# Kernel tuning notes

Hardware: AMD Instinct MI355X
Metric: run time of the kernel (lower is better)

Reference implementation:

```python
import jax, jax.numpy as jnp
import numpy as np
from math import pi, log

B, H, W, C = 8, 128, 128, 3
N_LAT, D_LAT = 256, 512
DEPTH = 4
NUM_BANDS = 6
MAX_FREQ = 10.0
BASE = 2.0
CROSS_HEADS, CROSS_DH = 1, 64
LAT_HEADS, LAT_DH = 8, 64
FF_MULT = 4
INPUT_DIM = 2 * (2 * NUM_BANDS + 1) + C  # 29


def setup_inputs():
    ki = iter(jax.random.split(jax.random.key(0), 40))

    def nrm(shape, s=0.02):
        return jax.random.normal(next(ki), shape, jnp.float32) * s

    ic, il = CROSS_HEADS * CROSS_DH, LAT_HEADS * LAT_DH
    d, q = DEPTH, INPUT_DIM
    return {
        "x": jax.random.normal(next(ki), (B, D_LAT), jnp.float32),
        "latents": jax.random.normal(next(ki), (N_LAT, D_LAT), jnp.float32),
        "W_l2l": nrm((D_LAT, N_LAT * D_LAT)),
        "b_l2l": jnp.zeros((N_LAT * D_LAT,), jnp.float32),
        "ca_ln_q_g": jnp.ones((d, q)), "ca_ln_q_b": jnp.zeros((d, q)),
        "ca_ln_c_g": jnp.ones((d, D_LAT)), "ca_ln_c_b": jnp.zeros((d, D_LAT)),
        "ca_Wq": nrm((d, q, ic)), "ca_Wkv": nrm((d, D_LAT, 2 * ic)),
        "ca_Wo": nrm((d, ic, q)), "ca_bo": jnp.zeros((d, q)),
        "cf_ln_g": jnp.ones((d, q)), "cf_ln_b": jnp.zeros((d, q)),
        "cf_W1": nrm((d, q, q * FF_MULT * 2)), "cf_b1": jnp.zeros((d, q * FF_MULT * 2)),
        "cf_W2": nrm((d, q * FF_MULT, q)), "cf_b2": jnp.zeros((d, q)),
        "la_ln_g": jnp.ones((d, D_LAT)), "la_ln_b": jnp.zeros((d, D_LAT)),
        "la_Wq": nrm((d, D_LAT, il)), "la_Wkv": nrm((d, D_LAT, 2 * il)),
        "la_Wo": nrm((d, il, D_LAT)), "la_bo": jnp.zeros((d, D_LAT)),
        "lf_ln_g": jnp.ones((d, D_LAT)), "lf_ln_b": jnp.zeros((d, D_LAT)),
        "lf_W1": nrm((d, D_LAT, D_LAT * FF_MULT * 2)), "lf_b1": jnp.zeros((d, D_LAT * FF_MULT * 2)),
        "lf_W2": nrm((d, D_LAT * FF_MULT, D_LAT)), "lf_b2": jnp.zeros((d, D_LAT)),
    }


def _ln(t, g, b):
    m = jnp.mean(t, -1, keepdims=True)
    v = jnp.mean(jnp.square(t - m), -1, keepdims=True)
    return (t - m) * jax.lax.rsqrt(v + 1e-5) * g + b


def _attn(xq, ctx, Wq, Wkv, Wo, bo, heads):
    dh = Wq.shape[-1] // heads
    b, n, _ = xq.shape
    m = ctx.shape[1]
    qh = (xq @ Wq).reshape(b, n, heads, dh)
    k, v = jnp.split(ctx @ Wkv, 2, axis=-1)
    kh = k.reshape(b, m, heads, dh)
    vh = v.reshape(b, m, heads, dh)
    sim = jnp.einsum('bihd,bjhd->bhij', qh, kh) * (dh ** -0.5)
    attn = jax.nn.softmax(sim, axis=-1)
    out = jnp.einsum('bhij,bjhd->bihd', attn, vh).reshape(b, n, heads * dh)
    return out @ Wo + bo


def _geglu_ff(t, W1, b1, W2, b2):
    a, g = jnp.split(t @ W1 + b1, 2, axis=-1)
    return (a * jax.nn.gelu(g, approximate=False)) @ W2 + b2


def _forward(x, latents, W_l2l, b_l2l, ca_ln_q_g, ca_ln_q_b, ca_ln_c_g, ca_ln_c_b,
             ca_Wq, ca_Wkv, ca_Wo, ca_bo, cf_ln_g, cf_ln_b, cf_W1, cf_b1, cf_W2, cf_b2,
             la_ln_g, la_ln_b, la_Wq, la_Wkv, la_Wo, la_bo,
             lf_ln_g, lf_ln_b, lf_W1, lf_b1, lf_W2, lf_b2):
    # expand latent code to a set of latents and add learned latent array
    lat = (x @ W_l2l + b_l2l).reshape(B, N_LAT, D_LAT) + latents  # (B, N, D)

    # Fourier positional encoding of the output grid
    pos = jnp.stack(jnp.meshgrid(jnp.linspace(-1.0, 1.0, H), jnp.linspace(-1.0, 1.0, W), indexing='ij'), axis=-1)  # (H, W, 2)
    scales = BASE ** jnp.linspace(1.0, log(MAX_FREQ / 2) / log(BASE), NUM_BANDS)  # torch.logspace
    xp = pos[..., None] * scales * pi  # (H, W, 2, NUM_BANDS)
    enc = jnp.concatenate([jnp.sin(xp), jnp.cos(xp), pos[..., None]], axis=-1)  # (H, W, 2, 2B+1)
    enc = enc.reshape(H, W, 2 * (2 * NUM_BANDS + 1)).astype(jnp.float32)

    data = jnp.concatenate([jnp.zeros((B, H, W, C), jnp.float32),
                            jnp.broadcast_to(enc, (B, H, W, enc.shape[-1]))], axis=-1)
    data = data.reshape(B, H * W, INPUT_DIM)

    for i in range(DEPTH):
        ln_lat = _ln(lat, la_ln_g[i], la_ln_b[i])
        lat = lat + _attn(ln_lat, ln_lat, la_Wq[i], la_Wkv[i], la_Wo[i], la_bo[i], LAT_HEADS)
        lat = lat + _geglu_ff(_ln(lat, lf_ln_g[i], lf_ln_b[i]), lf_W1[i], lf_b1[i], lf_W2[i], lf_b2[i])
        qn = _ln(data, ca_ln_q_g[i], ca_ln_q_b[i])
        cn = _ln(lat, ca_ln_c_g[i], ca_ln_c_b[i])
        data = data + _attn(qn, cn, ca_Wq[i], ca_Wkv[i], ca_Wo[i], ca_bo[i], CROSS_HEADS)
        data = data + _geglu_ff(_ln(data, cf_ln_g[i], cf_ln_b[i]), cf_W1[i], cf_b1[i], cf_W2[i], cf_b2[i])

    return data[..., :C].reshape(B, H, W, C)


def reference(x, latents, W_l2l, b_l2l, ca_ln_q_g, ca_ln_q_b, ca_ln_c_g, ca_ln_c_b,
              ca_Wq, ca_Wkv, ca_Wo, ca_bo, cf_ln_g, cf_ln_b, cf_W1, cf_b1, cf_W2, cf_b2,
              la_ln_g, la_ln_b, la_Wq, la_Wkv, la_Wo, la_bo,
              lf_ln_g, lf_ln_b, lf_W1, lf_b1, lf_W2, lf_b2):
    return _forward(x, latents, W_l2l, b_l2l, ca_ln_q_g, ca_ln_q_b, ca_ln_c_g, ca_ln_c_b,
                    ca_Wq, ca_Wkv, ca_Wo, ca_bo, cf_ln_g, cf_ln_b, cf_W1, cf_b1, cf_W2, cf_b2,
                    la_ln_g, la_ln_b, la_Wq, la_Wkv, la_Wo, la_bo,
                    lf_ln_g, lf_ln_b, lf_W1, lf_b1, lf_W2, lf_b2)
```

## Files before the change

kernel.cpp:

```cpp
#include <hip/hip_runtime.h>
#include <math.h>

#define DEV __device__ __forceinline__
#define LSTRIDE 8537088

DEV float gelu_exact(float x){ return 0.5f*x*(1.0f+erff(x*0.70710678118654752440f)); }

DEV unsigned short f2bf(float x){
  union { float f; unsigned int u; } v; v.f = x;
  unsigned int r = v.u + 0x7FFFu + ((v.u >> 16) & 1u);
  return (unsigned short)(r >> 16);
}
DEV float bf2f(unsigned short b){ union { unsigned int u; float f; } v; v.u = ((unsigned int)b)<<16; return v.f; }
DEV void split2(float x, unsigned short& h, unsigned short& l){
  h = f2bf(x); l = f2bf(x - bf2f(h));
}

typedef __bf16 bf16x8 __attribute__((ext_vector_type(8)));
typedef float  f32x4  __attribute__((ext_vector_type(4)));

DEV void gload16(const void* g, void* lds){
  __builtin_amdgcn_global_load_lds((const __attribute__((address_space(1))) unsigned int*)g,
                                   (__attribute__((address_space(3))) unsigned int*)lds, 16, 0, 0);
}

__global__ __launch_bounds__(256) void k_encode(float* __restrict__ data)
{
  int p = blockIdx.x*256 + threadIdx.x;
  int hh = p >> 7, ww = p & 127;
  float y = -1.0f + hh*(2.0f/127.0f);
  float x = -1.0f + ww*(2.0f/127.0f);
  float e[26];
  #pragma unroll
  for (int i=0;i<6;i++){
    float sc = exp2f(1.0f + i*0.26438561897747245f) * 3.14159265358979323846f;
    e[i]     = sinf(y*sc);
    e[6+i]   = cosf(y*sc);
    e[13+i]  = sinf(x*sc);
    e[19+i]  = cosf(x*sc);
  }
  e[12]=y; e[25]=x;
  #pragma unroll
  for (int b=0;b<8;b++){
    float* dr = data + ((size_t)(b*16384 + p))*29;
    dr[0]=0.f; dr[1]=0.f; dr[2]=0.f;
    #pragma unroll
    for (int c=0;c<26;c++) dr[3+c]=e[c];
  }
}

__global__ __launch_bounds__(256) void k_l2l(const float* __restrict__ x,
    const float* __restrict__ Wl, const float* __restrict__ bl,
    const float* __restrict__ latents, float* __restrict__ lat)
{
  __shared__ float xs[8*512];
  int tid = threadIdx.x;
  for (int idx=tid; idx<4096; idx+=256) xs[idx]=x[idx];
  __syncthreads();
  int nIdx = blockIdx.x*256 + tid;
  float acc[8] = {0,0,0,0,0,0,0,0};
  for (int k=0;k<512;k++){
    float w = Wl[(size_t)k*131072 + nIdx];
    #pragma unroll
    for (int m=0;m<8;m++) acc[m] += xs[m*512+k]*w;
  }
  float add = bl[nIdx] + latents[nIdx];
  #pragma unroll
  for (int m=0;m<8;m++) lat[(size_t)m*131072 + nIdx] = acc[m] + add;
}

__global__ __launch_bounds__(256) void k_ln512s(const float* __restrict__ X,
    const float* __restrict__ g, const float* __restrict__ bv,
    unsigned short* __restrict__ hi, unsigned short* __restrict__ lo)
{
  __shared__ float red[8];
  int row = blockIdx.x, tid = threadIdx.x;
  const float* x = X + (size_t)row*512;
  float v0 = x[tid], v1 = x[tid+256];
  float s = v0+v1;
  #pragma unroll
  for (int off=32; off; off>>=1) s += __shfl_xor(s, off);
  if ((tid&63)==0) red[tid>>6] = s;
  __syncthreads();
  float mean = (red[0]+red[1]+red[2]+red[3]) * (1.0f/512.0f);
  float d0 = v0-mean, d1 = v1-mean;
  float q = d0*d0 + d1*d1;
  #pragma unroll
  for (int off=32; off; off>>=1) q += __shfl_xor(q, off);
  if ((tid&63)==0) red[4+(tid>>6)] = q;
  __syncthreads();
  float var = (red[4]+red[5]+red[6]+red[7]) * (1.0f/512.0f);
  float rstd = rsqrtf(var + 1e-5f);
  float y0 = d0*rstd*g[tid]     + bv[tid];
  float y1 = d1*rstd*g[tid+256] + bv[tid+256];
  unsigned short h,l;
  split2(y0,h,l); hi[(size_t)row*512+tid]=h;     lo[(size_t)row*512+tid]=l;
  split2(y1,h,l); hi[(size_t)row*512+tid+256]=h; lo[(size_t)row*512+tid+256]=l;
}

__global__ __launch_bounds__(256) void k_split_w(const float* __restrict__ W,
    unsigned short* __restrict__ hi, int K, int N, int Ntot, int n0off)
{
  __shared__ float t[64][65];
  int z = blockIdx.z;
  W  += (size_t)z*K*N;
  hi += (size_t)z*LSTRIDE;
  unsigned short* lo = hi + (size_t)Ntot*K;
  int k0 = blockIdx.x*64, n0 = blockIdx.y*64;
  int tid = threadIdx.x;
  #pragma unroll
  for (int i=0;i<4;i++){
    int s = tid + 256*i;
    int r = s >> 4, c4 = (s & 15)*4;
    float4 v = *(const float4*)&W[(size_t)(k0+r)*N + n0 + c4];
    t[r][c4+0]=v.x; t[r][c4+1]=v.y; t[r][c4+2]=v.z; t[r][c4+3]=v.w;
  }
  __syncthreads();
  #pragma unroll
  for (int i=0;i<4;i++){
    int s = tid + 256*i;
    int n = s >> 4, kc = (s & 15)*4;
    size_t o = (size_t)(n0off + n0 + n)*K + k0 + kc;
    #pragma unroll
    for (int j=0;j<4;j++){
      unsigned short h,l; split2(t[kc+j][n], h, l);
      hi[o+j]=h; lo[o+j]=l;
    }
  }
}

__global__ __launch_bounds__(256) void k_prep_t(const float* __restrict__ src,
    unsigned short* __restrict__ dst, int K, int N, int Kd, int Nd)
{
  int z = blockIdx.z;
  src += (size_t)z*K*N;
  dst += (size_t)z*LSTRIDE;
  for (int idx = blockIdx.x*256 + threadIdx.x; idx < Nd*Kd; idx += gridDim.x*256){
    int n = idx / Kd, k = idx - n*Kd;
    float v = (k<K && n<N) ? src[(size_t)k*N + n] : 0.f;
    dst[idx] = f2bf(v);
  }
}

__global__ __launch_bounds__(256) void k_prep_w1(const float* __restrict__ W1,
    const float* __restrict__ b1, unsigned short* __restrict__ dst)
{
  int z = blockIdx.z;
  W1  += (size_t)z*6728;
  b1  += (size_t)z*232;
  dst += (size_t)z*LSTRIDE;
  float* b1r = (float*)(dst + 8192);
  for (int idx = blockIdx.x*256 + threadIdx.x; idx < 256*32; idx += gridDim.x*256){
    int n = idx >> 5, k = idx & 31;
    int f = n & 127, isg = n >> 7;
    float v = 0.f;
    if (f < 116 && k < 29) v = W1[(size_t)k*232 + isg*116 + f];
    dst[idx] = f2bf(v);
  }
  int n = blockIdx.x*256 + threadIdx.x;
  if (n < 256){
    int f = n & 127, isg = n >> 7;
    b1r[n] = (f < 116) ? b1[isg*116 + f] : 0.f;
  }
}

__global__ __launch_bounds__(256) void k_mfma(
    const unsigned short* __restrict__ Ahi, const unsigned short* __restrict__ Bhi,
    const float* __restrict__ bias, float* __restrict__ C,
    int M, int N, int K, int Ksplit, int accum)
{
  __shared__ unsigned short sm[4*128*32];
  int tid = threadIdx.x, lane = tid & 63, w = tid >> 6;
  int bm = blockIdx.x*128, bn = blockIdx.y*128;
  int Ks = K / Ksplit;
  int kbeg = blockIdx.z * Ks;
  const unsigned short* tsrc;
  if      (w==0) tsrc = Ahi + (size_t)bm*K;
  else if (w==1) tsrc = Ahi + (size_t)M*K + (size_t)bm*K;
  else if (w==2) tsrc = Bhi + (size_t)bn*K;
  else           tsrc = Bhi + (size_t)N*K + (size_t)bn*K;
  unsigned short* mylds = sm + w*4096;
  f32x4 acc[4][4];
  #pragma unroll
  for(int i=0;i<4;i++)
    #pragma unroll
    for(int j=0;j<4;j++) acc[i][j] = (f32x4){0.f,0.f,0.f,0.f};
  int wm = (w>>1)*64, wn = (w&1)*64;
  int frow = lane & 15, fq = lane >> 4;
  for (int k0 = kbeg; k0 < kbeg + Ks; k0 += 32){
    #pragma unroll
    for (int j=0;j<8;j++){
      int idx = j*64 + lane;
      int row = idx >> 2, qp = idx & 3;
      int q = (qp - row) & 3;
      gload16(tsrc + (size_t)row*K + k0 + q*8, mylds + j*512);
    }
    __syncthreads();
    bf16x8 ah[4], al[4];
    #pragma unroll
    for (int mt=0;mt<4;mt++){
      int row = wm + mt*16 + frow;
      int off = row*32 + ((fq + row)&3)*8;
      ah[mt] = *(const bf16x8*)(sm + off);
      al[mt] = *(const bf16x8*)(sm + 4096 + off);
    }
    #pragma unroll
    for (int nt=0;nt<4;nt++){
      int rowb = wn + nt*16 + frow;
      int offb = rowb*32 + ((fq + rowb)&3)*8;
      bf16x8 bh = *(const bf16x8*)(sm + 2*4096 + offb);
      bf16x8 bl = *(const bf16x8*)(sm + 3*4096 + offb);
      #pragma unroll
      for (int mt=0;mt<4;mt++){
        acc[mt][nt] = __builtin_amdgcn_mfma_f32_16x16x32_bf16(ah[mt], bh, acc[mt][nt], 0,0,0);
        acc[mt][nt] = __builtin_amdgcn_mfma_f32_16x16x32_bf16(ah[mt], bl, acc[mt][nt], 0,0,0);
        acc[mt][nt] = __builtin_amdgcn_mfma_f32_16x16x32_bf16(al[mt], bh, acc[mt][nt], 0,0,0);
      }
    }
    __syncthreads();
  }
  size_t zoff = (size_t)blockIdx.z * ((size_t)M*N);
  #pragma unroll
  for (int mt=0;mt<4;mt++){
    #pragma unroll
    for (int nt=0;nt<4;nt++){
      int col = bn + wn + nt*16 + frow;
      float bv = (bias && blockIdx.z==0) ? bias[col] : 0.f;
      #pragma unroll
      for (int r=0;r<4;r++){
        int row = bm + wm + mt*16 + fq*4 + r;
        float v = acc[mt][nt][r] + bv;
        if (accum) atomicAdd(&C[(size_t)row*N + col], v);
        else       C[zoff + (size_t)row*N + col] = v;
      }
    }
  }
}

__global__ __launch_bounds__(256) void k_mfma_qkv(
    const unsigned short* __restrict__ Ahi, const unsigned short* __restrict__ Bhi,
    float* __restrict__ qout, unsigned short* __restrict__ Kb,
    unsigned short* __restrict__ Vthi, unsigned short* __restrict__ Vtlo,
    int M, int N, int K)
{
  __shared__ unsigned short sm[4*128*32];
  int tid = threadIdx.x, lane = tid & 63, w = tid >> 6;
  int bm = blockIdx.x*128, bn = blockIdx.y*128;
  const unsigned short* tsrc;
  if      (w==0) tsrc = Ahi + (size_t)bm*K;
  else if (w==1) tsrc = Ahi + (size_t)M*K + (size_t)bm*K;
  else if (w==2) tsrc = Bhi + (size_t)bn*K;
  else           tsrc = Bhi + (size_t)N*K + (size_t)bn*K;
  unsigned short* mylds = sm + w*4096;
  f32x4 acc[4][4];
  #pragma unroll
  for(int i=0;i<4;i++)
    #pragma unroll
    for(int j=0;j<4;j++) acc[i][j] = (f32x4){0.f,0.f,0.f,0.f};
  int wm = (w>>1)*64, wn = (w&1)*64;
  int frow = lane & 15, fq = lane >> 4;
  for (int k0 = 0; k0 < K; k0 += 32){
    #pragma unroll
    for (int j=0;j<8;j++){
      int idx = j*64 + lane;
      int row = idx >> 2, qp = idx & 3;
      int q = (qp - row) & 3;
      gload16(tsrc + (size_t)row*K + k0 + q*8, mylds + j*512);
    }
    __syncthreads();
    bf16x8 ah[4], al[4];
    #pragma unroll
    for (int mt=0;mt<4;mt++){
      int row = wm + mt*16 + frow;
      int off = row*32 + ((fq + row)&3)*8;
      ah[mt] = *(const bf16x8*)(sm + off);
      al[mt] = *(const bf16x8*)(sm + 4096 + off);
    }
    #pragma unroll
    for (int nt=0;nt<4;nt++){
      int rowb = wn + nt*16 + frow;
      int offb = rowb*32 + ((fq + rowb)&3)*8;
      bf16x8 bh = *(const bf16x8*)(sm + 2*4096 + offb);
      bf16x8 bl = *(const bf16x8*)(sm + 3*4096 + offb);
      #pragma unroll
      for (int mt=0;mt<4;mt++){
        acc[mt][nt] = __builtin_amdgcn_mfma_f32_16x16x32_bf16(ah[mt], bh, acc[mt][nt], 0,0,0);
        acc[mt][nt] = __builtin_amdgcn_mfma_f32_16x16x32_bf16(ah[mt], bl, acc[mt][nt], 0,0,0);
        acc[mt][nt] = __builtin_amdgcn_mfma_f32_16x16x32_bf16(al[mt], bh, acc[mt][nt], 0,0,0);
      }
    }
    __syncthreads();
  }
  #pragma unroll
  for (int mt=0;mt<4;mt++){
    #pragma unroll
    for (int nt=0;nt<4;nt++){
      int col = bn + wn + nt*16 + frow;
      #pragma unroll
      for (int r=0;r<4;r++){
        int row = bm + wm + mt*16 + fq*4 + r;
        float v = acc[mt][nt][r];
        int b = row >> 8, j = row & 255;
        if (col < 512){
          qout[(size_t)row*512 + col] = v;
        } else if (col < 1024){
          int kc = col - 512, h = kc >> 6, d = kc & 63;
          Kb[((size_t)((b*8+h)*256 + j))*64 + d] = f2bf(v);
        } else {
          int vc = col - 1024, h = vc >> 6, d = vc & 63;
          size_t idx = ((size_t)((b*8+h)*64 + d))*256 + j;
          unsigned short hh,ll; split2(v,hh,ll);
          Vthi[idx]=hh; Vtlo[idx]=ll;
        }
      }
    }
  }
}

__global__ __launch_bounds__(256) void k_mfma_glu(
    const unsigned short* __restrict__ Ahi, const unsigned short* __restrict__ Whi,
    const float* __restrict__ b1, unsigned short* __restrict__ Ghi,
    unsigned short* __restrict__ Glo)
{
  __shared__ unsigned short sm[16384];
  int tid = threadIdx.x, lane = tid & 63, w = tid >> 6;
  int bm = blockIdx.x*128, bnp = blockIdx.y*64;
  const unsigned short* Alo = Ahi + (size_t)2048*512;
  const unsigned short* Wlo = Whi + (size_t)4096*512;
  f32x4 aa[4][2], ag[4][2];
  #pragma unroll
  for (int i=0;i<4;i++)
    #pragma unroll
    for (int j=0;j<2;j++){ aa[i][j]=(f32x4){0.f,0.f,0.f,0.f}; ag[i][j]=(f32x4){0.f,0.f,0.f,0.f}; }
  int wm = (w>>1)*64, wnp = (w&1)*32;
  int frow = lane & 15, fq = lane >> 4;
  for (int k0=0;k0<512;k0+=32){
    #pragma unroll
    for (int j=0;j<8;j++){
      int c0 = w*512 + j*64;
      int c  = c0 + lane;
      int sel = c0 >> 8;
      const unsigned short* src; int wi;
      if (sel < 4){
        src = (sel < 2 ? Ahi : Alo) + (size_t)bm*512;
        wi = c & 511;
      } else {
        const unsigned short* wb = (sel < 6) ? Whi : Wlo;
        int cb = bnp + ((sel & 1) ? 2048 : 0);
        src = wb + (size_t)cb*512;
        wi = c & 255;
      }
      int row = wi >> 2, qp = wi & 3;
      int q = (qp - row) & 3;
      gload16(src + (size_t)row*512 + k0 + q*8, sm + c0*8);
    }
    __syncthreads();
    bf16x8 ah[4], al[4];
    #pragma unroll
    for (int mt=0;mt<4;mt++){
      int r = wm + mt*16 + frow;
      int off = r*32 + ((fq + r)&3)*8;
      ah[mt] = *(const bf16x8*)(sm + off);
      al[mt] = *(const bf16x8*)(sm + 4096 + off);
    }
    #pragma unroll
    for (int nt=0;nt<2;nt++){
      int rb = wnp + nt*16 + frow;
      int offb = rb*32 + ((fq + rb)&3)*8;
      bf16x8 bah = *(const bf16x8*)(sm +  8192 + offb);
      bf16x8 bgh = *(const bf16x8*)(sm + 10240 + offb);
      bf16x8 bal = *(const bf16x8*)(sm + 12288 + offb);
      bf16x8 bgl = *(const bf16x8*)(sm + 14336 + offb);
      #pragma unroll
      for (int mt=0;mt<4;mt++){
        aa[mt][nt] = __builtin_amdgcn_mfma_f32_16x16x32_bf16(ah[mt], bah, aa[mt][nt], 0,0,0);
        aa[mt][nt] = __builtin_amdgcn_mfma_f32_16x16x32_bf16(ah[mt], bal, aa[mt][nt], 0,0,0);
        aa[mt][nt] = __builtin_amdgcn_mfma_f32_16x16x32_bf16(al[mt], bah, aa[mt][nt], 0,0,0);
        ag[mt][nt] = __builtin_amdgcn_mfma_f32_16x16x32_bf16(ah[mt], bgh, ag[mt][nt], 0,0,0);
        ag[mt][nt] = __builtin_amdgcn_mfma_f32_16x16x32_bf16(ah[mt], bgl, ag[mt][nt], 0,0,0);
        ag[mt][nt] = __builtin_amdgcn_mfma_f32_16x16x32_bf16(al[mt], bgh, ag[mt][nt], 0,0,0);
      }
    }
    __syncthreads();
  }
  #pragma unroll
  for (int mt=0;mt<4;mt++){
    #pragma unroll
    for (int nt=0;nt<2;nt++){
      int col = bnp + wnp + nt*16 + frow;
      float ba = b1[col], bg = b1[2048+col];
      #pragma unroll
      for (int r=0;r<4;r++){
        int row = bm + wm + mt*16 + fq*4 + r;
        float av = aa[mt][nt][r] + ba;
        float gv = ag[mt][nt][r] + bg;
        unsigned short h,l; split2(av*gelu_exact(gv), h, l);
        Ghi[(size_t)row*2048 + col] = h;
        Glo[(size_t)row*2048 + col] = l;
      }
    }
  }
}

__global__ __launch_bounds__(256) void k_kvprep(const float* __restrict__ kv, int ld,
    int koff, int voff, int heads, int BH,
    unsigned short* __restrict__ Kb, unsigned short* __restrict__ Vthi,
    unsigned short* __restrict__ Vtlo, int zparts, int zstride)
{
  int total = BH << 14;
  for (int idx = blockIdx.x*256 + threadIdx.x; idx < total; idx += gridDim.x*256){
    int d = idx & 63, j = (idx>>6) & 255, bh = idx >> 14;
    int b = bh / heads, h = bh - b*heads;
    size_t base = ((size_t)(b*256 + j))*ld + koff + h*64 + d;
    float v = 0.f;
    for (int z=0; z<zparts; z++) v += kv[(size_t)z*zstride + base];
    Kb[idx] = f2bf(v);
  }
  for (int idx = blockIdx.x*256 + threadIdx.x; idx < total; idx += gridDim.x*256){
    int j = idx & 255, d = (idx>>8) & 63, bh = idx >> 14;
    int b = bh / heads, h = bh - b*heads;
    size_t base = ((size_t)(b*256 + j))*ld + voff + h*64 + d;
    float v = 0.f;
    for (int z=0; z<zparts; z++) v += kv[(size_t)z*zstride + base];
    if (Vtlo){ unsigned short hh,ll; split2(v,hh,ll); Vthi[idx]=hh; Vtlo[idx]=ll; }
    else Vthi[idx] = f2bf(v);
  }
}

template<int QF32, int SPLITV, int OSPLIT>
__global__ __launch_bounds__(256) void k_attn_mf(
    const void* __restrict__ Qv, const unsigned short* __restrict__ Kb,
    const unsigned short* __restrict__ Vthi, const unsigned short* __restrict__ Vtlo,
    unsigned short* __restrict__ O0, unsigned short* __restrict__ O1,
    int q_rs, int o_rs, int heads, int nper, float scale)
{
  __shared__ unsigned short Pw[4*640];
  int tid = threadIdx.x, lane = tid & 63, w = tid >> 6;
  int l15 = lane & 15, g = lane >> 4;
  int bpb = nper >> 6;
  int bh = blockIdx.x / bpb;
  int q0 = (blockIdx.x - bh*bpb)*64 + w*16;
  int b = bh / heads, h = bh - b*heads;
  bf16x8 aq[2];
  int qrow = b*nper + q0 + l15;
  if (QF32){
    const float* qp = (const float*)Qv + (size_t)qrow*q_rs + h*64 + g*8;
    #pragma unroll
    for (int kt=0;kt<2;kt++){
      bf16x8 v;
      #pragma unroll
      for (int j=0;j<8;j++) v[j] = (__bf16)qp[kt*32 + j];
      aq[kt]=v;
    }
  } else {
    const unsigned short* qp = (const unsigned short*)Qv + (size_t)qrow*q_rs + h*64 + g*8;
    aq[0] = *(const bf16x8*)(qp);
    aq[1] = *(const bf16x8*)(qp + 32);
  }
  const unsigned short* kbb = Kb + ((size_t)bh*256 + l15)*64 + g*8;
  f32x4 sc[16];
  #pragma unroll
  for (int nt=0;nt<16;nt++) sc[nt] = (f32x4){0.f,0.f,0.f,0.f};
  #pragma unroll
  for (int nt=0;nt<16;nt++){
    bf16x8 b0 = *(const bf16x8*)(kbb + (size_t)nt*1024);
    bf16x8 b1 = *(const bf16x8*)(kbb + (size_t)nt*1024 + 32);
    sc[nt] = __builtin_amdgcn_mfma_f32_16x16x32_bf16(aq[0], b0, sc[nt], 0,0,0);
    sc[nt] = __builtin_amdgcn_mfma_f32_16x16x32_bf16(aq[1], b1, sc[nt], 0,0,0);
  }
  float mx[4] = {-1e30f,-1e30f,-1e30f,-1e30f};
  #pragma unroll
  for (int nt=0;nt<16;nt++)
    #pragma unroll
    for (int r=0;r<4;r++){ float v = sc[nt][r]*scale; sc[nt][r]=v; mx[r]=fmaxf(mx[r],v); }
  #pragma unroll
  for (int r=0;r<4;r++){
    #pragma unroll
    for (int m=1;m<16;m<<=1) mx[r] = fmaxf(mx[r], __shfl_xor(mx[r], m));
  }
  float sum[4] = {0.f,0.f,0.f,0.f};
  #pragma unroll
  for (int nt=0;nt<16;nt++)
    #pragma unroll
    for (int r=0;r<4;r++){ float e = __expf(sc[nt][r]-mx[r]); sc[nt][r]=e; sum[r]+=e; }
  #pragma unroll
  for (int r=0;r<4;r++){
    #pragma unroll
    for (int m=1;m<16;m<<=1) sum[r] += __shfl_xor(sum[r], m);
  }
  f32x4 o[4];
  #pragma unroll
  for (int nd=0;nd<4;nd++) o[nd] = (f32x4){0.f,0.f,0.f,0.f};
  unsigned short* pw = Pw + w*640;
  const unsigned short* vb  = Vthi + ((size_t)bh*64 + l15)*256 + g*8;
  const unsigned short* vbl = SPLITV ? (Vtlo + ((size_t)bh*64 + l15)*256 + g*8) : (const unsigned short*)0;
  #pragma unroll
  for (int kt=0;kt<8;kt++){
    __builtin_amdgcn_wave_barrier();
    #pragma unroll
    for (int t2=0;t2<2;t2++){
      int nt = kt*2 + t2;
      #pragma unroll
      for (int r=0;r<4;r++)
        pw[(g*4+r)*40 + t2*16 + l15] = f2bf(sc[nt][r]);
    }
    __builtin_amdgcn_wave_barrier();
    bf16x8 ap = *(const bf16x8*)(pw + l15*40 + g*8);
    #pragma unroll
    for (int nd=0;nd<4;nd++){
      bf16x8 bv = *(const bf16x8*)(vb + (size_t)nd*4096 + kt*32);
      o[nd] = __builtin_amdgcn_mfma_f32_16x16x32_bf16(ap, bv, o[nd], 0,0,0);
      if (SPLITV){
        bf16x8 bl = *(const bf16x8*)(vbl + (size_t)nd*4096 + kt*32);
        o[nd] = __builtin_amdgcn_mfma_f32_16x16x32_bf16(ap, bl, o[nd], 0,0,0);
      }
    }
  }
  float inv[4];
  #pragma unroll
  for (int r=0;r<4;r++) inv[r] = 1.0f/sum[r];
  int orow0 = b*nper + q0;
  #pragma unroll
  for (int nd=0;nd<4;nd++){
    #pragma unroll
    for (int r=0;r<4;r++){
      float v = o[nd][r]*inv[r];
      size_t off = (size_t)(orow0 + g*4 + r)*o_rs + h*64 + nd*16 + l15;
      if (OSPLIT){ unsigned short hh,ll; split2(v,hh,ll); O0[off]=hh; O1[off]=ll; }
      else O0[off] = f2bf(v);
    }
  }
}

__global__ __launch_bounds__(256) void k_cattn(
    const float* __restrict__ X, const float* __restrict__ lng, const float* __restrict__ lnb,
    const unsigned short* __restrict__ WqT, const unsigned short* __restrict__ Kb,
    const unsigned short* __restrict__ Vt, const unsigned short* __restrict__ WoT,
    const float* __restrict__ bo, float* __restrict__ C, float scale)
{
  __shared__ __align__(16) unsigned short qn[64*40];
  __shared__ __align__(16) unsigned short qa[4][16*72];
  int tid = threadIdx.x, lane = tid & 63, w = tid >> 6;
  int l15 = lane & 15, g = lane >> 4;
  int r0 = blockIdx.x*64;
  int bh = r0 >> 14;
  if (tid < 64){
    const float* x = X + (size_t)(r0 + tid)*29;
    float a[29]; float s = 0.f;
    #pragma unroll
    for (int k=0;k<29;k++){ a[k]=x[k]; s+=a[k]; }
    float mean = s*(1.0f/29.0f);
    float qv = 0.f;
    #pragma unroll
    for (int k=0;k<29;k++){ float d=a[k]-mean; qv+=d*d; }
    float rstd = rsqrtf(qv*(1.0f/29.0f) + 1e-5f);
    unsigned short yb[32] __attribute__((aligned(16)));
    #pragma unroll
    for (int k=0;k<29;k++) yb[k] = f2bf((a[k]-mean)*rstd*lng[k] + lnb[k]);
    yb[29]=0; yb[30]=0; yb[31]=0;
    uint4* d4 = (uint4*)(qn + tid*40);
    const uint4* s4 = (const uint4*)yb;
    d4[0]=s4[0]; d4[1]=s4[1]; d4[2]=s4[2]; d4[3]=s4[3];
  }
  __syncthreads();
  int rw = w*16;
  bf16x8 a0 = *(const bf16x8*)(qn + (rw + l15)*40 + g*8);
  f32x4 qv4[4];
  #pragma unroll
  for (int nt=0;nt<4;nt++) qv4[nt] = (f32x4){0.f,0.f,0.f,0.f};
  #pragma unroll
  for (int nt=0;nt<4;nt++){
    bf16x8 bw = *(const bf16x8*)(WqT + (size_t)(nt*16 + l15)*32 + g*8);
    qv4[nt] = __builtin_amdgcn_mfma_f32_16x16x32_bf16(a0, bw, qv4[nt], 0,0,0);
  }
  unsigned short* pa = qa[w];
  #pragma unroll
  for (int nt=0;nt<4;nt++)
    #pragma unroll
    for (int r=0;r<4;r++)
      pa[(g*4+r)*72 + nt*16 + l15] = f2bf(qv4[nt][r]);
  __builtin_amdgcn_wave_barrier();
  bf16x8 aq[2];
  aq[0] = *(const bf16x8*)(pa + l15*72 + g*8);
  aq[1] = *(const bf16x8*)(pa + l15*72 + 32 + g*8);
  __builtin_amdgcn_wave_barrier();
  const unsigned short* kbb = Kb + ((size_t)bh*256 + l15)*64 + g*8;
  f32x4 sc[16];
  #pragma unroll
  for (int nt=0;nt<16;nt++) sc[nt] = (f32x4){0.f,0.f,0.f,0.f};
  #pragma unroll
  for (int nt=0;nt<16;nt++){
    bf16x8 b0 = *(const bf16x8*)(kbb + (size_t)nt*1024);
    bf16x8 b1 = *(const bf16x8*)(kbb + (size_t)nt*1024 + 32);
    sc[nt] = __builtin_amdgcn_mfma_f32_16x16x32_bf16(aq[0], b0, sc[nt], 0,0,0);
    sc[nt] = __builtin_amdgcn_mfma_f32_16x16x32_bf16(aq[1], b1, sc[nt], 0,0,0);
  }
  float mx[4] = {-1e30f,-1e30f,-1e30f,-1e30f};
  #pragma unroll
  for (int nt=0;nt<16;nt++)
    #pragma unroll
    for (int r=0;r<4;r++){ float v = sc[nt][r]*scale; sc[nt][r]=v; mx[r]=fmaxf(mx[r],v); }
  #pragma unroll
  for (int r=0;r<4;r++){
    #pragma unroll
    for (int m=1;m<16;m<<=1) mx[r] = fmaxf(mx[r], __shfl_xor(mx[r], m));
  }
  float sum[4] = {0.f,0.f,0.f,0.f};
  #pragma unroll
  for (int nt=0;nt<16;nt++)
    #pragma unroll
    for (int r=0;r<4;r++){ float e = __expf(sc[nt][r]-mx[r]); sc[nt][r]=e; sum[r]+=e; }
  #pragma unroll
  for (int r=0;r<4;r++){
    #pragma unroll
    for (int m=1;m<16;m<<=1) sum[r] += __shfl_xor(sum[r], m);
  }
  f32x4 o[4];
  #pragma unroll
  for (int nd=0;nd<4;nd++) o[nd] = (f32x4){0.f,0.f,0.f,0.f};
  const unsigned short* vb = Vt + ((size_t)bh*64 + l15)*256 + g*8;
  #pragma unroll
  for (int kt=0;kt<8;kt++){
    __builtin_amdgcn_wave_barrier();
    #pragma unroll
    for (int t2=0;t2<2;t2++){
      int nt = kt*2 + t2;
      #pragma unroll
      for (int r=0;r<4;r++)
        pa[(g*4+r)*40 + t2*16 + l15] = f2bf(sc[nt][r]);
    }
    __builtin_amdgcn_wave_barrier();
    bf16x8 ap = *(const bf16x8*)(pa + l15*40 + g*8);
    #pragma unroll
    for (int nd=0;nd<4;nd++){
      bf16x8 bv = *(const bf16x8*)(vb + (size_t)nd*4096 + kt*32);
      o[nd] = __builtin_amdgcn_mfma_f32_16x16x32_bf16(ap, bv, o[nd], 0,0,0);
    }
  }
  float inv[4];
  #pragma unroll
  for (int r=0;r<4;r++) inv[r] = 1.0f/sum[r];
  __builtin_amdgcn_wave_barrier();
  #pragma unroll
  for (int nd=0;nd<4;nd++)
    #pragma unroll
    for (int r=0;r<4;r++)
      pa[(g*4+r)*72 + nd*16 + l15] = f2bf(o[nd][r]*inv[r]);
  __builtin_amdgcn_wave_barrier();
  bf16x8 ao0 = *(const bf16x8*)(pa + l15*72 + g*8);
  bf16x8 ao1 = *(const bf16x8*)(pa + l15*72 + 32 + g*8);
  f32x4 c2[2];
  #pragma unroll
  for (int nt=0;nt<2;nt++) c2[nt] = (f32x4){0.f,0.f,0.f,0.f};
  #pragma unroll
  for (int nt=0;nt<2;nt++){
    bf16x8 bw0 = *(const bf16x8*)(WoT + (size_t)(nt*16 + l15)*64 + g*8);
    bf16x8 bw1 = *(const bf16x8*)(WoT + (size_t)(nt*16 + l15)*64 + 32 + g*8);
    c2[nt] = __builtin_amdgcn_mfma_f32_16x16x32_bf16(ao0, bw0, c2[nt], 0,0,0);
    c2[nt] = __builtin_amdgcn_mfma_f32_16x16x32_bf16(ao1, bw1, c2[nt], 0,0,0);
  }
  #pragma unroll
  for (int nt=0;nt<2;nt++){
    int col = nt*16 + l15;
    if (col < 29){
      #pragma unroll
      for (int r=0;r<4;r++){
        size_t off = (size_t)(r0 + rw + g*4 + r)*29 + col;
        C[off] += c2[nt][r] + bo[col];
      }
    }
  }
}

__global__ __launch_bounds__(256) void k_cff(
    const float* __restrict__ X, const float* __restrict__ lng, const float* __restrict__ lnb,
    const unsigned short* __restrict__ W1rT, const float* __restrict__ b1r,
    const unsigned short* __restrict__ W2T, const float* __restrict__ b2,
    float* __restrict__ C)
{
  __shared__ __align__(16) unsigned short sm1[128*40];
  __shared__ __align__(16) unsigned short gga[4][32*136];
  int tid = threadIdx.x, lane = tid & 63, w = tid >> 6;
  int l15 = lane & 15, g = lane >> 4;
  int row0b = blockIdx.x*128;
  if (tid < 128){
    const float* x = X + (size_t)(row0b + tid)*29;
    float a[29]; float s = 0.f;
    #pragma unroll
    for (int k=0;k<29;k++){ a[k]=x[k]; s+=a[k]; }
    float mean = s*(1.0f/29.0f);
    float qv = 0.f;
    #pragma unroll
    for (int k=0;k<29;k++){ float d=a[k]-mean; qv+=d*d; }
    float rstd = rsqrtf(qv*(1.0f/29.0f) + 1e-5f);
    unsigned short yb[32] __attribute__((aligned(16)));
    #pragma unroll
    for (int k=0;k<29;k++) yb[k] = f2bf((a[k]-mean)*rstd*lng[k] + lnb[k]);
    yb[29]=0; yb[30]=0; yb[31]=0;
    uint4* d4 = (uint4*)(sm1 + tid*40);
    const uint4* s4 = (const uint4*)yb;
    d4[0]=s4[0]; d4[1]=s4[1]; d4[2]=s4[2]; d4[3]=s4[3];
  }
  __syncthreads();
  int rw = w*32;
  bf16x8 a0 = *(const bf16x8*)(sm1 + (rw + l15)*40 + g*8);
  bf16x8 a1 = *(const bf16x8*)(sm1 + (rw + 16 + l15)*40 + g*8);
  f32x4 acc[2][16];
  #pragma unroll
  for (int mt=0;mt<2;mt++)
    #pragma unroll
    for (int nt=0;nt<16;nt++) acc[mt][nt] = (f32x4){0.f,0.f,0.f,0.f};
  #pragma unroll
  for (int nt=0;nt<16;nt++){
    bf16x8 bw = *(const bf16x8*)(W1rT + (size_t)(nt*16 + l15)*32 + g*8);
    acc[0][nt] = __builtin_amdgcn_mfma_f32_16x16x32_bf16(a0, bw, acc[0][nt], 0,0,0);
    acc[1][nt] = __builtin_amdgcn_mfma_f32_16x16x32_bf16(a1, bw, acc[1][nt], 0,0,0);
  }
  unsigned short* gg = gga[w];
  #pragma unroll
  for (int mt=0;mt<2;mt++){
    #pragma unroll
    for (int t=0;t<8;t++){
      float ba = b1r[t*16 + l15];
      float bg = b1r[128 + t*16 + l15];
      #pragma unroll
      for (int r=0;r<4;r++){
        float av = acc[mt][t][r]   + ba;
        float gv = acc[mt][t+8][r] + bg;
        gg[(mt*16 + g*4 + r)*136 + t*16 + l15] = f2bf(av * gelu_exact(gv));
      }
    }
  }
  __builtin_amdgcn_wave_barrier();
  f32x4 c2[2][2];
  #pragma unroll
  for (int mt=0;mt<2;mt++)
    #pragma unroll
    for (int nt=0;nt<2;nt++) c2[mt][nt] = (f32x4){0.f,0.f,0.f,0.f};
  #pragma unroll
  for (int kt=0;kt<4;kt++){
    bf16x8 af0 = *(const bf16x8*)(gg + (size_t)(l15)*136 + kt*32 + g*8);
    bf16x8 af1 = *(const bf16x8*)(gg + (size_t)(16 + l15)*136 + kt*32 + g*8);
    #pragma unroll
    for (int nt=0;nt<2;nt++){
      bf16x8 bw = *(const bf16x8*)(W2T + (size_t)(nt*16 + l15)*128 + kt*32 + g*8);
      c2[0][nt] = __builtin_amdgcn_mfma_f32_16x16x32_bf16(af0, bw, c2[0][nt], 0,0,0);
      c2[1][nt] = __builtin_amdgcn_mfma_f32_16x16x32_bf16(af1, bw, c2[1][nt], 0,0,0);
    }
  }
  #pragma unroll
  for (int mt=0;mt<2;mt++)
    #pragma unroll
    for (int nt=0;nt<2;nt++){
      int col = nt*16 + l15;
      if (col < 29){
        #pragma unroll
        for (int r=0;r<4;r++){
          size_t off = (size_t)(row0b + rw + mt*16 + g*4 + r)*29 + col;
          C[off] += c2[mt][nt][r] + b2[col];
        }
      }
    }
}

__global__ __launch_bounds__(256) void k_out(const float* __restrict__ data, float* __restrict__ out)
{
  int idx = blockIdx.x*256 + threadIdx.x;
  int p = idx/3, c = idx - p*3;
  out[idx] = data[(size_t)p*29 + c];
}

extern "C" void kernel_launch(void* const* d_in, const int* in_sizes, int n_in,
                              void* d_out, int out_size, void* d_ws, size_t ws_size,
                              hipStream_t stream) {
  const float* x        = (const float*)d_in[0];
  const float* latents  = (const float*)d_in[1];
  const float* W_l2l    = (const float*)d_in[2];
  const float* b_l2l    = (const float*)d_in[3];
  const float* ca_ln_q_g= (const float*)d_in[4];
  const float* ca_ln_q_b= (const float*)d_in[5];
  const float* ca_ln_c_g= (const float*)d_in[6];
  const float* ca_ln_c_b= (const float*)d_in[7];
  const float* ca_Wq    = (const float*)d_in[8];
  const float* ca_Wkv   = (const float*)d_in[9];
  const float* ca_Wo    = (const float*)d_in[10];
  const float* ca_bo    = (const float*)d_in[11];
  const float* cf_ln_g  = (const float*)d_in[12];
  const float* cf_ln_b  = (const float*)d_in[13];
  const float* cf_W1    = (const float*)d_in[14];
  const float* cf_b1    = (const float*)d_in[15];
  const float* cf_W2    = (const float*)d_in[16];
  const float* cf_b2    = (const float*)d_in[17];
  const float* la_ln_g  = (const float*)d_in[18];
  const float* la_ln_b  = (const float*)d_in[19];
  const float* la_Wq    = (const float*)d_in[20];
  const float* la_Wkv   = (const float*)d_in[21];
  const float* la_Wo    = (const float*)d_in[22];
  const float* la_bo    = (const float*)d_in[23];
  const float* lf_ln_g  = (const float*)d_in[24];
  const float* lf_ln_b  = (const float*)d_in[25];
  const float* lf_W1    = (const float*)d_in[26];
  const float* lf_b1    = (const float*)d_in[27];
  const float* lf_W2    = (const float*)d_in[28];
  const float* lf_b2    = (const float*)d_in[29];

  float* ws = (float*)d_ws;
  float* data = ws;
  float* lat  = ws + 3801088;
  unsigned short* latn_hi = (unsigned short*)(ws + 4849664);
  unsigned short* latn_lo = latn_hi + 1048576;
  float* I    = ws + 5898240;
  float* kv_c = ws + 20578304;
  unsigned short* Kb_c = (unsigned short*)(ws + 21626880);
  unsigned short* Vt_c = Kb_c + 131072;
  unsigned short* wsp  = (unsigned short*)(ws + 21757952);
  float* q_l  = I;
  unsigned short* Kb_l   = (unsigned short*)(I + 3145728);
  unsigned short* Vthi_l = Kb_l + 1048576;
  unsigned short* Vtlo_l = Vthi_l + 1048576;
  unsigned short* ao_hi  = (unsigned short*)(I + 4718592);
  unsigned short* ao_lo  = ao_hi + 1048576;
  unsigned short* gg_hi = (unsigned short*)(I + 8388608);
  unsigned short* gg_lo = gg_hi + 4194304;

  k_encode<<<64, 256, 0, stream>>>(data);
  k_l2l   <<<512, 256, 0, stream>>>(x, W_l2l, b_l2l, latents, lat);

  k_split_w<<<dim3(8,8,4),  256,0,stream>>>(la_Wq,  wsp,          512, 512, 1536, 0);
  k_split_w<<<dim3(8,16,4), 256,0,stream>>>(la_Wkv, wsp,          512,1024, 1536, 512);
  k_split_w<<<dim3(8,8,4),  256,0,stream>>>(la_Wo,  wsp+1572864,  512, 512,  512, 0);
  k_split_w<<<dim3(8,64,4), 256,0,stream>>>(lf_W1,  wsp+2097152,  512,4096, 4096, 0);
  k_split_w<<<dim3(32,8,4), 256,0,stream>>>(lf_W2,  wsp+6291456, 2048, 512,  512, 0);
  k_split_w<<<dim3(8,2,4),  256,0,stream>>>(ca_Wkv, wsp+8388608,  512, 128,  128, 0);
  k_prep_t <<<dim3(4,1,4),256,0,stream>>>(ca_Wq, wsp+8519680, 29, 64, 32, 64);
  k_prep_t <<<dim3(4,1,4),256,0,stream>>>(ca_Wo, wsp+8521728, 64, 29, 64, 32);
  k_prep_t <<<dim3(8,1,4),256,0,stream>>>(cf_W2, wsp+8523776, 116, 29, 128, 32);
  k_prep_w1<<<dim3(32,1,4),256,0,stream>>>(cf_W1, cf_b1, wsp+8527872);

  for (int i=0;i<4;i++){
    unsigned short* wl = wsp + (size_t)i*LSTRIDE;
    unsigned short* wqkvt= wl;
    unsigned short* wot  = wl + 1572864;
    unsigned short* w1t  = wl + 2097152;
    unsigned short* w2t  = wl + 6291456;
    unsigned short* cakvt= wl + 8388608;
    unsigned short* WqT  = wl + 8519680;
    unsigned short* WoT  = wl + 8521728;
    unsigned short* W2T  = wl + 8523776;
    unsigned short* W1rT = wl + 8527872;
    float* b1r = (float*)(wl + 8536064);

    k_ln512s<<<2048,256,0,stream>>>(lat, la_ln_g+i*512, la_ln_b+i*512, latn_hi, latn_lo);
    k_mfma_qkv<<<dim3(16,12),256,0,stream>>>(latn_hi, wqkvt, q_l, Kb_l, Vthi_l, Vtlo_l,
                                             2048, 1536, 512);
    k_attn_mf<1,1,1><<<256,256,0,stream>>>(q_l, Kb_l, Vthi_l, Vtlo_l, ao_hi, ao_lo,
                                           512, 512, 8, 256, 0.125f);
    k_mfma<<<dim3(16,4,2),256,0,stream>>>(ao_hi, wot, la_bo+i*512, lat, 2048, 512, 512, 2, 1);
    k_ln512s<<<2048,256,0,stream>>>(lat, lf_ln_g+i*512, lf_ln_b+i*512, latn_hi, latn_lo);
    k_mfma_glu<<<dim3(16,32),256,0,stream>>>(latn_hi, w1t, lf_b1+i*4096, gg_hi, gg_lo);
    k_mfma<<<dim3(16,4,4),256,0,stream>>>(gg_hi, w2t, lf_b2+i*512, lat, 2048, 512, 2048, 4, 1);
    k_ln512s<<<2048,256,0,stream>>>(lat, ca_ln_c_g+i*512, ca_ln_c_b+i*512, latn_hi, latn_lo);
    k_mfma<<<dim3(16,1,4),256,0,stream>>>(latn_hi, cakvt, nullptr, kv_c, 2048, 128, 512, 4, 0);
    k_kvprep<<<512,256,0,stream>>>(kv_c, 128, 0, 64, 1, 8, Kb_c, Vt_c, nullptr, 4, 262144);
    k_cattn<<<2048,256,0,stream>>>(data, ca_ln_q_g+i*29, ca_ln_q_b+i*29, WqT,
                                   Kb_c, Vt_c, WoT, ca_bo+i*29, data, 0.125f);
    k_cff<<<1024,256,0,stream>>>(data, cf_ln_g+i*29, cf_ln_b+i*29, W1rT, b1r,
                                 W2T, cf_b2+i*29, data);
  }

  k_out<<<1536,256,0,stream>>>(data, (float*)d_out);
}
```

Baseline: 1.863 ms.

## Merge independent stages into combo kernels and skew cross-attention one layer behind

```diff
diff --git a/kernel.cpp b/kernel.cpp
--- a/kernel.cpp
+++ b/kernel.cpp
@@ -24,9 +24,9 @@
                                    (__attribute__((address_space(3))) unsigned int*)lds, 16, 0, 0);
 }
 
-__global__ __launch_bounds__(256) void k_encode(float* __restrict__ data)
-{
-  int p = blockIdx.x*256 + threadIdx.x;
+DEV void dev_encode(int bx, float* __restrict__ data, int tid)
+{
+  int p = bx*256 + tid;
   int hh = p >> 7, ww = p & 127;
   float y = -1.0f + hh*(2.0f/127.0f);
   float x = -1.0f + ww*(2.0f/127.0f);
@@ -49,15 +49,13 @@
   }
 }
 
-__global__ __launch_bounds__(256) void k_l2l(const float* __restrict__ x,
+DEV void dev_l2l(int bx, float* xs, const float* __restrict__ x,
     const float* __restrict__ Wl, const float* __restrict__ bl,
-    const float* __restrict__ latents, float* __restrict__ lat)
-{
-  __shared__ float xs[8*512];
-  int tid = threadIdx.x;
+    const float* __restrict__ latents, float* __restrict__ lat, int tid)
+{
   for (int idx=tid; idx<4096; idx+=256) xs[idx]=x[idx];
   __syncthreads();
-  int nIdx = blockIdx.x*256 + tid;
+  int nIdx = bx*256 + tid;
   float acc[8] = {0,0,0,0,0,0,0,0};
   for (int k=0;k<512;k++){
     float w = Wl[(size_t)k*131072 + nIdx];
@@ -69,51 +67,19 @@
   for (int m=0;m<8;m++) lat[(size_t)m*131072 + nIdx] = acc[m] + add;
 }
 
-__global__ __launch_bounds__(256) void k_ln512s(const float* __restrict__ X,
-    const float* __restrict__ g, const float* __restrict__ bv,
-    unsigned short* __restrict__ hi, unsigned short* __restrict__ lo)
-{
-  __shared__ float red[8];
-  int row = blockIdx.x, tid = threadIdx.x;
-  const float* x = X + (size_t)row*512;
-  float v0 = x[tid], v1 = x[tid+256];
-  float s = v0+v1;
-  #pragma unroll
-  for (int off=32; off; off>>=1) s += __shfl_xor(s, off);
-  if ((tid&63)==0) red[tid>>6] = s;
-  __syncthreads();
-  float mean = (red[0]+red[1]+red[2]+red[3]) * (1.0f/512.0f);
-  float d0 = v0-mean, d1 = v1-mean;
-  float q = d0*d0 + d1*d1;
-  #pragma unroll
-  for (int off=32; off; off>>=1) q += __shfl_xor(q, off);
-  if ((tid&63)==0) red[4+(tid>>6)] = q;
-  __syncthreads();
-  float var = (red[4]+red[5]+red[6]+red[7]) * (1.0f/512.0f);
-  float rstd = rsqrtf(var + 1e-5f);
-  float y0 = d0*rstd*g[tid]     + bv[tid];
-  float y1 = d1*rstd*g[tid+256] + bv[tid+256];
-  unsigned short h,l;
-  split2(y0,h,l); hi[(size_t)row*512+tid]=h;     lo[(size_t)row*512+tid]=l;
-  split2(y1,h,l); hi[(size_t)row*512+tid+256]=h; lo[(size_t)row*512+tid+256]=l;
-}
-
-__global__ __launch_bounds__(256) void k_split_w(const float* __restrict__ W,
-    unsigned short* __restrict__ hi, int K, int N, int Ntot, int n0off)
-{
-  __shared__ float t[64][65];
-  int z = blockIdx.z;
+DEV void dev_split_w(int bx, int by, int z, float* t, const float* __restrict__ W,
+    unsigned short* __restrict__ hi, int K, int N, int Ntot, int n0off, int tid)
+{
   W  += (size_t)z*K*N;
   hi += (size_t)z*LSTRIDE;
   unsigned short* lo = hi + (size_t)Ntot*K;
-  int k0 = blockIdx.x*64, n0 = blockIdx.y*64;
-  int tid = threadIdx.x;
+  int k0 = bx*64, n0 = by*64;
   #pragma unroll
   for (int i=0;i<4;i++){
     int s = tid + 256*i;
     int r = s >> 4, c4 = (s & 15)*4;
     float4 v = *(const float4*)&W[(size_t)(k0+r)*N + n0 + c4];
-    t[r][c4+0]=v.x; t[r][c4+1]=v.y; t[r][c4+2]=v.z; t[r][c4+3]=v.w;
+    t[r*65+c4+0]=v.x; t[r*65+c4+1]=v.y; t[r*65+c4+2]=v.z; t[r*65+c4+3]=v.w;
   }
   __syncthreads();
   #pragma unroll
@@ -123,57 +89,54 @@
     size_t o = (size_t)(n0off + n0 + n)*K + k0 + kc;
     #pragma unroll
     for (int j=0;j<4;j++){
-      unsigned short h,l; split2(t[kc+j][n], h, l);
+      unsigned short h,l; split2(t[(kc+j)*65+n], h, l);
       hi[o+j]=h; lo[o+j]=l;
     }
   }
 }
 
-__global__ __launch_bounds__(256) void k_prep_t(const float* __restrict__ src,
-    unsigned short* __restrict__ dst, int K, int N, int Kd, int Nd)
-{
-  int z = blockIdx.z;
+DEV void dev_prep_t(int bx, int z, int nbx, const float* __restrict__ src,
+    unsigned short* __restrict__ dst, int K, int N, int Kd, int Nd, int tid)
+{
   src += (size_t)z*K*N;
   dst += (size_t)z*LSTRIDE;
-  for (int idx = blockIdx.x*256 + threadIdx.x; idx < Nd*Kd; idx += gridDim.x*256){
+  for (int idx = bx*256 + tid; idx < Nd*Kd; idx += nbx*256){
     int n = idx / Kd, k = idx - n*Kd;
     float v = (k<K && n<N) ? src[(size_t)k*N + n] : 0.f;
     dst[idx] = f2bf(v);
   }
 }
 
-__global__ __launch_bounds__(256) void k_prep_w1(const float* __restrict__ W1,
-    const float* __restrict__ b1, unsigned short* __restrict__ dst)
-{
-  int z = blockIdx.z;
+DEV void dev_prep_w1(int bx, int z, const float* __restrict__ W1,
+    const float* __restrict__ b1, unsigned short* __restrict__ dst, int tid)
+{
   W1  += (size_t)z*6728;
   b1  += (size_t)z*232;
   dst += (size_t)z*LSTRIDE;
   float* b1r = (float*)(dst + 8192);
-  for (int idx = blockIdx.x*256 + threadIdx.x; idx < 256*32; idx += gridDim.x*256){
+  for (int idx = bx*256 + tid; idx < 256*32; idx += 32*256){
     int n = idx >> 5, k = idx & 31;
     int f = n & 127, isg = n >> 7;
     float v = 0.f;
     if (f < 116 && k < 29) v = W1[(size_t)k*232 + isg*116 + f];
     dst[idx] = f2bf(v);
   }
-  int n = blockIdx.x*256 + threadIdx.x;
+  int n = bx*256 + tid;
   if (n < 256){
     int f = n & 127, isg = n >> 7;
     b1r[n] = (f < 116) ? b1[isg*116 + f] : 0.f;
   }
 }
 
-__global__ __launch_bounds__(256) void k_mfma(
+DEV void dev_gemm(int bx, int by, int bz, unsigned short* sm,
     const unsigned short* __restrict__ Ahi, const unsigned short* __restrict__ Bhi,
     const float* __restrict__ bias, float* __restrict__ C,
-    int M, int N, int K, int Ksplit, int accum)
-{
-  __shared__ unsigned short sm[4*128*32];
-  int tid = threadIdx.x, lane = tid & 63, w = tid >> 6;
-  int bm = blockIdx.x*128, bn = blockIdx.y*128;
+    int M, int N, int K, int Ksplit, int accum, int tid)
+{
+  int lane = tid & 63, w = tid >> 6;
+  int bm = bx*128, bn = by*128;
   int Ks = K / Ksplit;
-  int kbeg = blockIdx.z * Ks;
+  int kbeg = bz * Ks;
   const unsigned short* tsrc;
   if      (w==0) tsrc = Ahi + (size_t)bm*K;
   else if (w==1) tsrc = Ahi + (size_t)M*K + (size_t)bm*K;
@@ -219,13 +182,13 @@
     }
     __syncthreads();
   }
-  size_t zoff = (size_t)blockIdx.z * ((size_t)M*N);
+  size_t zoff = (size_t)bz * ((size_t)M*N);
   #pragma unroll
   for (int mt=0;mt<4;mt++){
     #pragma unroll
     for (int nt=0;nt<4;nt++){
       int col = bn + wn + nt*16 + frow;
-      float bv = (bias && blockIdx.z==0) ? bias[col] : 0.f;
+      float bv = (bias && bz==0) ? bias[col] : 0.f;
       #pragma unroll
       for (int r=0;r<4;r++){
         int row = bm + wm + mt*16 + fq*4 + r;
@@ -237,15 +200,14 @@
   }
 }
 
-__global__ __launch_bounds__(256) void k_mfma_qkv(
+DEV void dev_qkv(int bx, int by, unsigned short* sm,
     const unsigned short* __restrict__ Ahi, const unsigned short* __restrict__ Bhi,
     float* __restrict__ qout, unsigned short* __restrict__ Kb,
-    unsigned short* __restrict__ Vthi, unsigned short* __restrict__ Vtlo,
-    int M, int N, int K)
-{
-  __shared__ unsigned short sm[4*128*32];
-  int tid = threadIdx.x, lane = tid & 63, w = tid >> 6;
-  int bm = blockIdx.x*128, bn = blockIdx.y*128;
+    unsigned short* __restrict__ Vthi, unsigned short* __restrict__ Vtlo, int tid)
+{
+  const int M = 2048, N = 1536, K = 512;
+  int lane = tid & 63, w = tid >> 6;
+  int bm = bx*128, bn = by*128;
   const unsigned short* tsrc;
   if      (w==0) tsrc = Ahi + (size_t)bm*K;
   else if (w==1) tsrc = Ahi + (size_t)M*K + (size_t)bm*K;
@@ -317,12 +279,529 @@
   }
 }
 
+DEV void dev_attn(int bid, unsigned short* Pw,
+    const float* __restrict__ Qv, const unsigned short* __restrict__ Kb,
+    const unsigned short* __restrict__ Vthi, const unsigned short* __restrict__ Vtlo,
+    unsigned short* __restrict__ O0, unsigned short* __restrict__ O1,
+    int q_rs, int o_rs, int heads, int nper, float scale, int tid)
+{
+  int lane = tid & 63, w = tid >> 6;
+  int l15 = lane & 15, g = lane >> 4;
+  int bpb = nper >> 6;
+  int bh = bid / bpb;
+  int q0 = (bid - bh*bpb)*64 + w*16;
+  int b = bh / heads, h = bh - b*heads;
+  bf16x8 aq[2];
+  int qrow = b*nper + q0 + l15;
+  const float* qp = Qv + (size_t)qrow*q_rs + h*64 + g*8;
+  #pragma unroll
+  for (int kt=0;kt<2;kt++){
+    bf16x8 v;
+    #pragma unroll
+    for (int j=0;j<8;j++) v[j] = (__bf16)qp[kt*32 + j];
+    aq[kt]=v;
+  }
+  const unsigned short* kbb = Kb + ((size_t)bh*256 + l15)*64 + g*8;
+  f32x4 sc[16];
+  #pragma unroll
+  for (int nt=0;nt<16;nt++) sc[nt] = (f32x4){0.f,0.f,0.f,0.f};
+  #pragma unroll
+  for (int nt=0;nt<16;nt++){
+    bf16x8 b0 = *(const bf16x8*)(kbb + (size_t)nt*1024);
+    bf16x8 b1 = *(const bf16x8*)(kbb + (size_t)nt*1024 + 32);
+    sc[nt] = __builtin_amdgcn_mfma_f32_16x16x32_bf16(aq[0], b0, sc[nt], 0,0,0);
+    sc[nt] = __builtin_amdgcn_mfma_f32_16x16x32_bf16(aq[1], b1, sc[nt], 0,0,0);
+  }
+  float mx[4] = {-1e30f,-1e30f,-1e30f,-1e30f};
+  #pragma unroll
+  for (int nt=0;nt<16;nt++)
+    #pragma unroll
+    for (int r=0;r<4;r++){ float v = sc[nt][r]*scale; sc[nt][r]=v; mx[r]=fmaxf(mx[r],v); }
+  #pragma unroll
+  for (int r=0;r<4;r++){
+    #pragma unroll
+    for (int m=1;m<16;m<<=1) mx[r] = fmaxf(mx[r], __shfl_xor(mx[r], m));
+  }
+  float sum[4] = {0.f,0.f,0.f,0.f};
+  #pragma unroll
+  for (int nt=0;nt<16;nt++)
+    #pragma unroll
+    for (int r=0;r<4;r++){ float e = __expf(sc[nt][r]-mx[r]); sc[nt][r]=e; sum[r]+=e; }
+  #pragma unroll
+  for (int r=0;r<4;r++){
+    #pragma unroll
+    for (int m=1;m<16;m<<=1) sum[r] += __shfl_xor(sum[r], m);
+  }
+  f32x4 o[4];
+  #pragma unroll
+  for (int nd=0;nd<4;nd++) o[nd] = (f32x4){0.f,0.f,0.f,0.f};
+  unsigned short* pw = Pw + w*640;
+  const unsigned short* vb  = Vthi + ((size_t)bh*64 + l15)*256 + g*8;
+  const unsigned short* vbl = Vtlo + ((size_t)bh*64 + l15)*256 + g*8;
+  #pragma unroll
+  for (int kt=0;kt<8;kt++){
+    __builtin_amdgcn_wave_barrier();
+    #pragma unroll
+    for (int t2=0;t2<2;t2++){
+      int nt = kt*2 + t2;
+      #pragma unroll
+      for (int r=0;r<4;r++)
+        pw[(g*4+r)*40 + t2*16 + l15] = f2bf(sc[nt][r]);
+    }
+    __builtin_amdgcn_wave_barrier();
+    bf16x8 ap = *(const bf16x8*)(pw + l15*40 + g*8);
+    #pragma unroll
+    for (int nd=0;nd<4;nd++){
+      bf16x8 bv = *(const bf16x8*)(vb + (size_t)nd*4096 + kt*32);
+      o[nd] = __builtin_amdgcn_mfma_f32_16x16x32_bf16(ap, bv, o[nd], 0,0,0);
+      bf16x8 bl = *(const bf16x8*)(vbl + (size_t)nd*4096 + kt*32);
+      o[nd] = __builtin_amdgcn_mfma_f32_16x16x32_bf16(ap, bl, o[nd], 0,0,0);
+    }
+  }
+  float inv[4];
+  #pragma unroll
+  for (int r=0;r<4;r++) inv[r] = 1.0f/sum[r];
+  int orow0 = b*nper + q0;
+  #pragma unroll
+  for (int nd=0;nd<4;nd++){
+    #pragma unroll
+    for (int r=0;r<4;r++){
+      float v = o[nd][r]*inv[r];
+      size_t off = (size_t)(orow0 + g*4 + r)*o_rs + h*64 + nd*16 + l15;
+      unsigned short hh,ll; split2(v,hh,ll); O0[off]=hh; O1[off]=ll;
+    }
+  }
+}
+
+DEV void dev_kvprep(int bid, int nb, const float* __restrict__ kv, int ld,
+    int koff, int voff, int heads, int BH,
+    unsigned short* __restrict__ Kb, unsigned short* __restrict__ Vthi,
+    int zparts, int zstride, int tid)
+{
+  int total = BH << 14;
+  for (int idx = bid*256 + tid; idx < total; idx += nb*256){
+    int d = idx & 63, j = (idx>>6) & 255, bh = idx >> 14;
+    int b = bh / heads, h = bh - b*heads;
+    size_t base = ((size_t)(b*256 + j))*ld + koff + h*64 + d;
+    float v = 0.f;
+    for (int z=0; z<zparts; z++) v += kv[(size_t)z*zstride + base];
+    Kb[idx] = f2bf(v);
+  }
+  for (int idx = bid*256 + tid; idx < total; idx += nb*256){
+    int j = idx & 255, d = (idx>>8) & 63, bh = idx >> 14;
+    int b = bh / heads, h = bh - b*heads;
+    size_t base = ((size_t)(b*256 + j))*ld + voff + h*64 + d;
+    float v = 0.f;
+    for (int z=0; z<zparts; z++) v += kv[(size_t)z*zstride + base];
+    Vthi[idx] = f2bf(v);
+  }
+}
+
+DEV void dev_cattn(int bid, unsigned short* smb,
+    const float* __restrict__ X, const float* __restrict__ lng, const float* __restrict__ lnb,
+    const unsigned short* __restrict__ WqT, const unsigned short* __restrict__ Kb,
+    const unsigned short* __restrict__ Vt, const unsigned short* __restrict__ WoT,
+    const float* __restrict__ bo, float* __restrict__ C, float scale, int tid)
+{
+  unsigned short* qn = smb;
+  unsigned short* qa = smb + 2560;
+  int lane = tid & 63, w = tid >> 6;
+  int l15 = lane & 15, g = lane >> 4;
+  int r0 = bid*64;
+  int bh = r0 >> 14;
+  if (tid < 64){
+    const float* x = X + (size_t)(r0 + tid)*29;
+    float a[29]; float s = 0.f;
+    #pragma unroll
+    for (int k=0;k<29;k++){ a[k]=x[k]; s+=a[k]; }
+    float mean = s*(1.0f/29.0f);
+    float qv = 0.f;
+    #pragma unroll
+    for (int k=0;k<29;k++){ float d=a[k]-mean; qv+=d*d; }
+    float rstd = rsqrtf(qv*(1.0f/29.0f) + 1e-5f);
+    unsigned short yb[32] __attribute__((aligned(16)));
+    #pragma unroll
+    for (int k=0;k<29;k++) yb[k] = f2bf((a[k]-mean)*rstd*lng[k] + lnb[k]);
+    yb[29]=0; yb[30]=0; yb[31]=0;
+    uint4* d4 = (uint4*)(qn + tid*40);
+    const uint4* s4 = (const uint4*)yb;
+    d4[0]=s4[0]; d4[1]=s4[1]; d4[2]=s4[2]; d4[3]=s4[3];
+  }
+  __syncthreads();
+  int rw = w*16;
+  bf16x8 a0 = *(const bf16x8*)(qn + (rw + l15)*40 + g*8);
+  f32x4 qv4[4];
+  #pragma unroll
+  for (int nt=0;nt<4;nt++) qv4[nt] = (f32x4){0.f,0.f,0.f,0.f};
+  #pragma unroll
+  for (int nt=0;nt<4;nt++){
+    bf16x8 bw = *(const bf16x8*)(WqT + (size_t)(nt*16 + l15)*32 + g*8);
+    qv4[nt] = __builtin_amdgcn_mfma_f32_16x16x32_bf16(a0, bw, qv4[nt], 0,0,0);
+  }
+  unsigned short* pa = qa + w*1152;
+  #pragma unroll
+  for (int nt=0;nt<4;nt++)
+    #pragma unroll
+    for (int r=0;r<4;r++)
+      pa[(g*4+r)*72 + nt*16 + l15] = f2bf(qv4[nt][r]);
+  __builtin_amdgcn_wave_barrier();
+  bf16x8 aq[2];
+  aq[0] = *(const bf16x8*)(pa + l15*72 + g*8);
+  aq[1] = *(const bf16x8*)(pa + l15*72 + 32 + g*8);
+  __builtin_amdgcn_wave_barrier();
+  const unsigned short* kbb = Kb + ((size_t)bh*256 + l15)*64 + g*8;
+  f32x4 sc[16];
+  #pragma unroll
+  for (int nt=0;nt<16;nt++) sc[nt] = (f32x4){0.f,0.f,0.f,0.f};
+  #pragma unroll
+  for (int nt=0;nt<16;nt++){
+    bf16x8 b0 = *(const bf16x8*)(kbb + (size_t)nt*1024);
+    bf16x8 b1 = *(const bf16x8*)(kbb + (size_t)nt*1024 + 32);
+    sc[nt] = __builtin_amdgcn_mfma_f32_16x16x32_bf16(aq[0], b0, sc[nt], 0,0,0);
+    sc[nt] = __builtin_amdgcn_mfma_f32_16x16x32_bf16(aq[1], b1, sc[nt], 0,0,0);
+  }
+  float mx[4] = {-1e30f,-1e30f,-1e30f,-1e30f};
+  #pragma unroll
+  for (int nt=0;nt<16;nt++)
+    #pragma unroll
+    for (int r=0;r<4;r++){ float v = sc[nt][r]*scale; sc[nt][r]=v; mx[r]=fmaxf(mx[r],v); }
+  #pragma unroll
+  for (int r=0;r<4;r++){
+    #pragma unroll
+    for (int m=1;m<16;m<<=1) mx[r] = fmaxf(mx[r], __shfl_xor(mx[r], m));
+  }
+  float sum[4] = {0.f,0.f,0.f,0.f};
+  #pragma unroll
+  for (int nt=0;nt<16;nt++)
+    #pragma unroll
+    for (int r=0;r<4;r++){ float e = __expf(sc[nt][r]-mx[r]); sc[nt][r]=e; sum[r]+=e; }
+  #pragma unroll
+  for (int r=0;r<4;r++){
+    #pragma unroll
+    for (int m=1;m<16;m<<=1) sum[r] += __shfl_xor(sum[r], m);
+  }
+  f32x4 o[4];
+  #pragma unroll
+  for (int nd=0;nd<4;nd++) o[nd] = (f32x4){0.f,0.f,0.f,0.f};
+  const unsigned short* vb = Vt + ((size_t)bh*64 + l15)*256 + g*8;
+  #pragma unroll
+  for (int kt=0;kt<8;kt++){
+    __builtin_amdgcn_wave_barrier();
+    #pragma unroll
+    for (int t2=0;t2<2;t2++){
+      int nt = kt*2 + t2;
+      #pragma unroll
+      for (int r=0;r<4;r++)
+        pa[(g*4+r)*40 + t2*16 + l15] = f2bf(sc[nt][r]);
+    }
+    __builtin_amdgcn_wave_barrier();
+    bf16x8 ap = *(const bf16x8*)(pa + l15*40 + g*8);
+    #pragma unroll
+    for (int nd=0;nd<4;nd++){
+      bf16x8 bv = *(const bf16x8*)(vb + (size_t)nd*4096 + kt*32);
+      o[nd] = __builtin_amdgcn_mfma_f32_16x16x32_bf16(ap, bv, o[nd], 0,0,0);
+    }
+  }
+  float inv[4];
+  #pragma unroll
+  for (int r=0;r<4;r++) inv[r] = 1.0f/sum[r];
+  __builtin_amdgcn_wave_barrier();
+  #pragma unroll
+  for (int nd=0;nd<4;nd++)
+    #pragma unroll
+    for (int r=0;r<4;r++)
+      pa[(g*4+r)*72 + nd*16 + l15] = f2bf(o[nd][r]*inv[r]);
+  __builtin_amdgcn_wave_barrier();
+  bf16x8 ao0 = *(const bf16x8*)(pa + l15*72 + g*8);
+  bf16x8 ao1 = *(const bf16x8*)(pa + l15*72 + 32 + g*8);
+  f32x4 c2[2];
+  #pragma unroll
+  for (int nt=0;nt<2;nt++) c2[nt] = (f32x4){0.f,0.f,0.f,0.f};
+  #pragma unroll
+  for (int nt=0;nt<2;nt++){
+    bf16x8 bw0 = *(const bf16x8*)(WoT + (size_t)(nt*16 + l15)*64 + g*8);
+    bf16x8 bw1 = *(const bf16x8*)(WoT + (size_t)(nt*16 + l15)*64 + 32 + g*8);
+    c2[nt] = __builtin_amdgcn_mfma_f32_16x16x32_bf16(ao0, bw0, c2[nt], 0,0,0);
+    c2[nt] = __builtin_amdgcn_mfma_f32_16x16x32_bf16(ao1, bw1, c2[nt], 0,0,0);
+  }
+  #pragma unroll
+  for (int nt=0;nt<2;nt++){
+    int col = nt*16 + l15;
+    if (col < 29){
+      #pragma unroll
+      for (int r=0;r<4;r++){
+        size_t off = (size_t)(r0 + rw + g*4 + r)*29 + col;
+        C[off] += c2[nt][r] + bo[col];
+      }
+    }
+  }
+}
+
+DEV void dev_cff(int bid, unsigned short* smb,
+    const float* __restrict__ X, const float* __restrict__ lng, const float* __restrict__ lnb,
+    const unsigned short* __restrict__ W1rT, const float* __restrict__ b1r,
+    const unsigned short* __restrict__ W2T, const float* __restrict__ b2,
+    float* __restrict__ C, int tid)
+{
+  unsigned short* sm1 = smb;
+  unsigned short* gga = smb + 5120;
+  int lane = tid & 63, w = tid >> 6;
+  int l15 = lane & 15, g = lane >> 4;
+  int row0b = bid*128;
+  if (tid < 128){
+    const float* x = X + (size_t)(row0b + tid)*29;
+    float a[29]; float s = 0.f;
+    #pragma unroll
+    for (int k=0;k<29;k++){ a[k]=x[k]; s+=a[k]; }
+    float mean = s*(1.0f/29.0f);
+    float qv = 0.f;
+    #pragma unroll
+    for (int k=0;k<29;k++){ float d=a[k]-mean; qv+=d*d; }
+    float rstd = rsqrtf(qv*(1.0f/29.0f) + 1e-5f);
+    unsigned short yb[32] __attribute__((aligned(16)));
+    #pragma unroll
+    for (int k=0;k<29;k++) yb[k] = f2bf((a[k]-mean)*rstd*lng[k] + lnb[k]);
+    yb[29]=0; yb[30]=0; yb[31]=0;
+    uint4* d4 = (uint4*)(sm1 + tid*40);
+    const uint4* s4 = (const uint4*)yb;
+    d4[0]=s4[0]; d4[1]=s4[1]; d4[2]=s4[2]; d4[3]=s4[3];
+  }
+  __syncthreads();
+  int rw = w*32;
+  bf16x8 a0 = *(const bf16x8*)(sm1 + (rw + l15)*40 + g*8);
+  bf16x8 a1 = *(const bf16x8*)(sm1 + (rw + 16 + l15)*40 + g*8);
+  f32x4 acc[2][16];
+  #pragma unroll
+  for (int mt=0;mt<2;mt++)
+    #pragma unroll
+    for (int nt=0;nt<16;nt++) acc[mt][nt] = (f32x4){0.f,0.f,0.f,0.f};
+  #pragma unroll
+  for (int nt=0;nt<16;nt++){
+    bf16x8 bw = *(const bf16x8*)(W1rT + (size_t)(nt*16 + l15)*32 + g*8);
+    acc[0][nt] = __builtin_amdgcn_mfma_f32_16x16x32_bf16(a0, bw, acc[0][nt], 0,0,0);
+    acc[1][nt] = __builtin_amdgcn_mfma_f32_16x16x32_bf16(a1, bw, acc[1][nt], 0,0,0);
+  }
+  unsigned short* gg = gga + w*4352;
+  #pragma unroll
+  for (int mt=0;mt<2;mt++){
+    #pragma unroll
+    for (int t=0;t<8;t++){
+      float ba = b1r[t*16 + l15];
+      float bg = b1r[128 + t*16 + l15];
+      #pragma unroll
+      for (int r=0;r<4;r++){
+        float av = acc[mt][t][r]   + ba;
+        float gv = acc[mt][t+8][r] + bg;
+        gg[(mt*16 + g*4 + r)*136 + t*16 + l15] = f2bf(av * gelu_exact(gv));
+      }
+    }
+  }
+  __builtin_amdgcn_wave_barrier();
+  f32x4 c2[2][2];
+  #pragma unroll
+  for (int mt=0;mt<2;mt++)
+    #pragma unroll
+    for (int nt=0;nt<2;nt++) c2[mt][nt] = (f32x4){0.f,0.f,0.f,0.f};
+  #pragma unroll
+  for (int kt=0;kt<4;kt++){
+    bf16x8 af0 = *(const bf16x8*)(gg + (size_t)(l15)*136 + kt*32 + g*8);
+    bf16x8 af1 = *(const bf16x8*)(gg + (size_t)(16 + l15)*136 + kt*32 + g*8);
+    #pragma unroll
+    for (int nt=0;nt<2;nt++){
+      bf16x8 bw = *(const bf16x8*)(W2T + (size_t)(nt*16 + l15)*128 + kt*32 + g*8);
+      c2[0][nt] = __builtin_amdgcn_mfma_f32_16x16x32_bf16(af0, bw, c2[0][nt], 0,0,0);
+      c2[1][nt] = __builtin_amdgcn_mfma_f32_16x16x32_bf16(af1, bw, c2[1][nt], 0,0,0);
+    }
+  }
+  #pragma unroll
+  for (int mt=0;mt<2;mt++)
+    #pragma unroll
+    for (int nt=0;nt<2;nt++){
+      int col = nt*16 + l15;
+      if (col < 29){
+        #pragma unroll
+        for (int r=0;r<4;r++){
+          size_t off = (size_t)(row0b + rw + mt*16 + g*4 + r)*29 + col;
+          C[off] += c2[mt][nt][r] + b2[col];
+        }
+      }
+    }
+}
+
+DEV void ln512_stats(const float* __restrict__ X, int row, int lane, float a[8],
+                     float& mean, float& rstd)
+{
+  const float* x = X + (size_t)row*512 + lane*8;
+  float4 v0 = *(const float4*)x;
+  float4 v1 = *(const float4*)(x+4);
+  a[0]=v0.x; a[1]=v0.y; a[2]=v0.z; a[3]=v0.w;
+  a[4]=v1.x; a[5]=v1.y; a[6]=v1.z; a[7]=v1.w;
+  float s = (a[0]+a[1])+(a[2]+a[3])+((a[4]+a[5])+(a[6]+a[7]));
+  #pragma unroll
+  for (int off=32; off; off>>=1) s += __shfl_xor(s, off);
+  mean = s * (1.0f/512.0f);
+  float q = 0.f;
+  #pragma unroll
+  for (int j=0;j<8;j++){ float d=a[j]-mean; q += d*d; }
+  #pragma unroll
+  for (int off=32; off; off>>=1) q += __shfl_xor(q, off);
+  rstd = rsqrtf(q*(1.0f/512.0f) + 1e-5f);
+}
+DEV void ln512_apply(const float a[8], float mean, float rstd,
+    const float* __restrict__ g, const float* __restrict__ bv, int row, int lane,
+    unsigned short* __restrict__ hi, unsigned short* __restrict__ lo)
+{
+  const float* gp = g + lane*8; const float* bp = bv + lane*8;
+  float4 g0=*(const float4*)gp, g1=*(const float4*)(gp+4);
+  float4 b0=*(const float4*)bp, b1=*(const float4*)(bp+4);
+  float gg[8]={g0.x,g0.y,g0.z,g0.w,g1.x,g1.y,g1.z,g1.w};
+  float bb[8]={b0.x,b0.y,b0.z,b0.w,b1.x,b1.y,b1.z,b1.w};
+  unsigned short hb[8] __attribute__((aligned(16)));
+  unsigned short lb[8] __attribute__((aligned(16)));
+  #pragma unroll
+  for (int j=0;j<8;j++){
+    unsigned short h,l; split2((a[j]-mean)*rstd*gg[j]+bb[j],h,l);
+    hb[j]=h; lb[j]=l;
+  }
+  *(uint4*)(hi + (size_t)row*512 + lane*8) = *(const uint4*)hb;
+  *(uint4*)(lo + (size_t)row*512 + lane*8) = *(const uint4*)lb;
+}
+DEV void dev_ln512w(int bid, const float* __restrict__ X,
+    const float* __restrict__ g, const float* __restrict__ bv,
+    unsigned short* __restrict__ hi, unsigned short* __restrict__ lo, int tid)
+{
+  int w = tid>>6, lane = tid&63;
+  int row = bid*4 + w;
+  float a[8], mean, rstd;
+  ln512_stats(X, row, lane, a, mean, rstd);
+  ln512_apply(a, mean, rstd, g, bv, row, lane, hi, lo);
+}
+
+__global__ __launch_bounds__(256) void k_prep_all(
+    const float* __restrict__ x, const float* __restrict__ Wl, const float* __restrict__ bl,
+    const float* __restrict__ latents, float* __restrict__ lat, float* __restrict__ data,
+    const float* __restrict__ la_Wq, const float* __restrict__ la_Wkv, const float* __restrict__ la_Wo,
+    const float* __restrict__ lf_W1, const float* __restrict__ lf_W2, const float* __restrict__ ca_Wkv,
+    const float* __restrict__ ca_Wq, const float* __restrict__ ca_Wo, const float* __restrict__ cf_W2,
+    const float* __restrict__ cf_W1, const float* __restrict__ cf_b1,
+    unsigned short* __restrict__ wsp)
+{
+  __shared__ __align__(16) float smf[4160];
+  int b = blockIdx.x, tid = threadIdx.x;
+  if (b < 512){ dev_l2l(b, smf, x, Wl, bl, latents, lat, tid); return; }
+  b -= 512;
+  if (b < 2048){ dev_split_w(b%8, (b/8)%64, b/512, smf, lf_W1, wsp+2097152, 512,4096,4096,0, tid); return; }
+  b -= 2048;
+  if (b < 1024){ dev_split_w(b%32, (b/32)%8, b/256, smf, lf_W2, wsp+6291456, 2048,512,512,0, tid); return; }
+  b -= 1024;
+  if (b < 512){ dev_split_w(b%8, (b/8)%16, b/128, smf, la_Wkv, wsp, 512,1024,1536,512, tid); return; }
+  b -= 512;
+  if (b < 256){ dev_split_w(b%8, (b/8)%8, b/64, smf, la_Wq, wsp, 512,512,1536,0, tid); return; }
+  b -= 256;
+  if (b < 256){ dev_split_w(b%8, (b/8)%8, b/64, smf, la_Wo, wsp+1572864, 512,512,512,0, tid); return; }
+  b -= 256;
+  if (b < 64){ dev_encode(b, data, tid); return; }
+  b -= 64;
+  if (b < 64){ dev_split_w(b%8, (b/8)%2, b/16, smf, ca_Wkv, wsp+8388608, 512,128,128,0, tid); return; }
+  b -= 64;
+  if (b < 128){ dev_prep_w1(b%32, b/32, cf_W1, cf_b1, wsp+8527872, tid); return; }
+  b -= 128;
+  if (b < 16){ dev_prep_t(b%4, b/4, 4, ca_Wq, wsp+8519680, 29,64,32,64, tid); return; }
+  b -= 16;
+  if (b < 16){ dev_prep_t(b%4, b/4, 4, ca_Wo, wsp+8521728, 64,29,64,32, tid); return; }
+  b -= 16;
+  dev_prep_t(b%8, b/8, 8, cf_W2, wsp+8523776, 116,29,128,32, tid);
+}
+
+__global__ __launch_bounds__(256) void k_ln512w(const float* __restrict__ X,
+    const float* __restrict__ g, const float* __restrict__ bv,
+    unsigned short* __restrict__ hi, unsigned short* __restrict__ lo)
+{
+  dev_ln512w(blockIdx.x, X, g, bv, hi, lo, threadIdx.x);
+}
+
+__global__ __launch_bounds__(256) void k_ln512d(const float* __restrict__ X,
+    const float* __restrict__ g1, const float* __restrict__ b1v,
+    unsigned short* __restrict__ h1, unsigned short* __restrict__ l1,
+    const float* __restrict__ g2, const float* __restrict__ b2v,
+    unsigned short* __restrict__ h2, unsigned short* __restrict__ l2)
+{
+  int tid = threadIdx.x, w = tid>>6, lane = tid&63;
+  int row = blockIdx.x*4 + w;
+  float a[8], mean, rstd;
+  ln512_stats(X, row, lane, a, mean, rstd);
+  ln512_apply(a, mean, rstd, g1, b1v, row, lane, h1, l1);
+  ln512_apply(a, mean, rstd, g2, b2v, row, lane, h2, l2);
+}
+
+__global__ __launch_bounds__(256) void k_combo1(
+    const unsigned short* __restrict__ Aq, const unsigned short* __restrict__ Wqkv,
+    float* __restrict__ q_l, unsigned short* __restrict__ Kb_l,
+    unsigned short* __restrict__ Vthi_l, unsigned short* __restrict__ Vtlo_l,
+    const unsigned short* __restrict__ Ac, const unsigned short* __restrict__ Wckv,
+    float* __restrict__ kv_c, int nA)
+{
+  __shared__ __align__(16) unsigned short sm[16384];
+  int b = blockIdx.x, tid = threadIdx.x;
+  if (b < nA) dev_qkv(b%16, b/16, sm, Aq, Wqkv, q_l, Kb_l, Vthi_l, Vtlo_l, tid);
+  else { int c = b - nA; dev_gemm(c%16, 0, c/16, sm, Ac, Wckv, nullptr, kv_c, 2048,128,512,4,0, tid); }
+}
+
+__global__ __launch_bounds__(256) void k_combo2(
+    const float* __restrict__ q_l, const unsigned short* __restrict__ Kb_l,
+    const unsigned short* __restrict__ Vthi_l, const unsigned short* __restrict__ Vtlo_l,
+    unsigned short* __restrict__ ao_hi, unsigned short* __restrict__ ao_lo,
+    const float* __restrict__ kv_c, unsigned short* __restrict__ Kb_c,
+    unsigned short* __restrict__ Vt_c, int nA, int nB)
+{
+  __shared__ __align__(16) unsigned short Pw[2560];
+  int b = blockIdx.x, tid = threadIdx.x;
+  if (b < nA) dev_attn(b, Pw, q_l, Kb_l, Vthi_l, Vtlo_l, ao_hi, ao_lo, 512, 512, 8, 256, 0.125f, tid);
+  else dev_kvprep(b - nA, nB, kv_c, 128, 0, 64, 1, 8, Kb_c, Vt_c, 4, 262144, tid);
+}
+
+__global__ __launch_bounds__(256) void k_combo3(
+    const unsigned short* __restrict__ ao_hi, const unsigned short* __restrict__ wot,
+    const float* __restrict__ bo_l, float* __restrict__ lat,
+    float* __restrict__ data, const float* __restrict__ lng, const float* __restrict__ lnb,
+    const unsigned short* __restrict__ WqT, const unsigned short* __restrict__ Kb_c,
+    const unsigned short* __restrict__ Vt_c, const unsigned short* __restrict__ WoT,
+    const float* __restrict__ bo_c, int nA)
+{
+  __shared__ __align__(16) unsigned short sm[16384];
+  int b = blockIdx.x, tid = threadIdx.x;
+  if (b < nA) dev_gemm(b%16, (b/16)%4, b/64, sm, ao_hi, wot, bo_l, lat, 2048,512,512,2,1, tid);
+  else dev_cattn(b - nA, sm, data, lng, lnb, WqT, Kb_c, Vt_c, WoT, bo_c, data, 0.125f, tid);
+}
+
+__global__ __launch_bounds__(256) void k_combo4(
+    float* __restrict__ data, const float* __restrict__ cf_g, const float* __restrict__ cf_b,
+    const unsigned short* __restrict__ W1rT, const float* __restrict__ b1r,
+    const unsigned short* __restrict__ W2T, const float* __restrict__ b2c,
+    const float* __restrict__ lat, const float* __restrict__ lf_g, const float* __restrict__ lf_b,
+    unsigned short* __restrict__ lnf_hi, unsigned short* __restrict__ lnf_lo, int nA)
+{
+  __shared__ __align__(16) unsigned short sm[22528];
+  int b = blockIdx.x, tid = threadIdx.x;
+  if (b < nA) dev_cff(b, sm, data, cf_g, cf_b, W1rT, b1r, W2T, b2c, data, tid);
+  else dev_ln512w(b - nA, lat, lf_g, lf_b, lnf_hi, lnf_lo, tid);
+}
+
+__global__ __launch_bounds__(256) void k_mfma(
+    const unsigned short* __restrict__ Ahi, const unsigned short* __restrict__ Bhi,
+    const float* __restrict__ bias, float* __restrict__ C,
+    int M, int N, int K, int Ksplit, int accum)
+{
+  __shared__ __align__(16) unsigned short sm[16384];
+  dev_gemm(blockIdx.x, blockIdx.y, blockIdx.z, sm, Ahi, Bhi, bias, C, M, N, K, Ksplit, accum, threadIdx.x);
+}
+
 __global__ __launch_bounds__(256) void k_mfma_glu(
     const unsigned short* __restrict__ Ahi, const unsigned short* __restrict__ Whi,
     const float* __restrict__ b1, unsigned short* __restrict__ Ghi,
     unsigned short* __restrict__ Glo)
 {
-  __shared__ unsigned short sm[16384];
+  __shared__ __align__(16) unsigned short sm[16384];
   int tid = threadIdx.x, lane = tid & 63, w = tid >> 6;
   int bm = blockIdx.x*128, bnp = blockIdx.y*64;
   const unsigned short* Alo = Ahi + (size_t)2048*512;
@@ -400,367 +879,6 @@
       }
     }
   }
-}
-
-__global__ __launch_bounds__(256) void k_kvprep(const float* __restrict__ kv, int ld,
-    int koff, int voff, int heads, int BH,
-    unsigned short* __restrict__ Kb, unsigned short* __restrict__ Vthi,
-    unsigned short* __restrict__ Vtlo, int zparts, int zstride)
-{
-  int total = BH << 14;
-  for (int idx = blockIdx.x*256 + threadIdx.x; idx < total; idx += gridDim.x*256){
-    int d = idx & 63, j = (idx>>6) & 255, bh = idx >> 14;
-    int b = bh / heads, h = bh - b*heads;
-    size_t base = ((size_t)(b*256 + j))*ld + koff + h*64 + d;
-    float v = 0.f;
-    for (int z=0; z<zparts; z++) v += kv[(size_t)z*zstride + base];
-    Kb[idx] = f2bf(v);
-  }
-  for (int idx = blockIdx.x*256 + threadIdx.x; idx < total; idx += gridDim.x*256){
-    int j = idx & 255, d = (idx>>8) & 63, bh = idx >> 14;
-    int b = bh / heads, h = bh - b*heads;
-    size_t base = ((size_t)(b*256 + j))*ld + voff + h*64 + d;
-    float v = 0.f;
-    for (int z=0; z<zparts; z++) v += kv[(size_t)z*zstride + base];
-    if (Vtlo){ unsigned short hh,ll; split2(v,hh,ll); Vthi[idx]=hh; Vtlo[idx]=ll; }
-    else Vthi[idx] = f2bf(v);
-  }
-}
-
-template<int QF32, int SPLITV, int OSPLIT>
-__global__ __launch_bounds__(256) void k_attn_mf(
-    const void* __restrict__ Qv, const unsigned short* __restrict__ Kb,
-    const unsigned short* __restrict__ Vthi, const unsigned short* __restrict__ Vtlo,
-    unsigned short* __restrict__ O0, unsigned short* __restrict__ O1,
-    int q_rs, int o_rs, int heads, int nper, float scale)
-{
-  __shared__ unsigned short Pw[4*640];
-  int tid = threadIdx.x, lane = tid & 63, w = tid >> 6;
-  int l15 = lane & 15, g = lane >> 4;
-  int bpb = nper >> 6;
-  int bh = blockIdx.x / bpb;
-  int q0 = (blockIdx.x - bh*bpb)*64 + w*16;
-  int b = bh / heads, h = bh - b*heads;
-  bf16x8 aq[2];
-  int qrow = b*nper + q0 + l15;
-  if (QF32){
-    const float* qp = (const float*)Qv + (size_t)qrow*q_rs + h*64 + g*8;
-    #pragma unroll
-    for (int kt=0;kt<2;kt++){
-      bf16x8 v;
-      #pragma unroll
-      for (int j=0;j<8;j++) v[j] = (__bf16)qp[kt*32 + j];
-      aq[kt]=v;
-    }
-  } else {
-    const unsigned short* qp = (const unsigned short*)Qv + (size_t)qrow*q_rs + h*64 + g*8;
-    aq[0] = *(const bf16x8*)(qp);
-    aq[1] = *(const bf16x8*)(qp + 32);
-  }
-  const unsigned short* kbb = Kb + ((size_t)bh*256 + l15)*64 + g*8;
-  f32x4 sc[16];
-  #pragma unroll
-  for (int nt=0;nt<16;nt++) sc[nt] = (f32x4){0.f,0.f,0.f,0.f};
-  #pragma unroll
-  for (int nt=0;nt<16;nt++){
-    bf16x8 b0 = *(const bf16x8*)(kbb + (size_t)nt*1024);
-    bf16x8 b1 = *(const bf16x8*)(kbb + (size_t)nt*1024 + 32);
-    sc[nt] = __builtin_amdgcn_mfma_f32_16x16x32_bf16(aq[0], b0, sc[nt], 0,0,0);
-    sc[nt] = __builtin_amdgcn_mfma_f32_16x16x32_bf16(aq[1], b1, sc[nt], 0,0,0);
-  }
-  float mx[4] = {-1e30f,-1e30f,-1e30f,-1e30f};
-  #pragma unroll
-  for (int nt=0;nt<16;nt++)
-    #pragma unroll
-    for (int r=0;r<4;r++){ float v = sc[nt][r]*scale; sc[nt][r]=v; mx[r]=fmaxf(mx[r],v); }
-  #pragma unroll
-  for (int r=0;r<4;r++){
-    #pragma unroll
-    for (int m=1;m<16;m<<=1) mx[r] = fmaxf(mx[r], __shfl_xor(mx[r], m));
-  }
-  float sum[4] = {0.f,0.f,0.f,0.f};
-  #pragma unroll
-  for (int nt=0;nt<16;nt++)
-    #pragma unroll
-    for (int r=0;r<4;r++){ float e = __expf(sc[nt][r]-mx[r]); sc[nt][r]=e; sum[r]+=e; }
-  #pragma unroll
-  for (int r=0;r<4;r++){
-    #pragma unroll
-    for (int m=1;m<16;m<<=1) sum[r] += __shfl_xor(sum[r], m);
-  }
-  f32x4 o[4];
-  #pragma unroll
-  for (int nd=0;nd<4;nd++) o[nd] = (f32x4){0.f,0.f,0.f,0.f};
-  unsigned short* pw = Pw + w*640;
-  const unsigned short* vb  = Vthi + ((size_t)bh*64 + l15)*256 + g*8;
-  const unsigned short* vbl = SPLITV ? (Vtlo + ((size_t)bh*64 + l15)*256 + g*8) : (const unsigned short*)0;
-  #pragma unroll
-  for (int kt=0;kt<8;kt++){
-    __builtin_amdgcn_wave_barrier();
-    #pragma unroll
-    for (int t2=0;t2<2;t2++){
-      int nt = kt*2 + t2;
-      #pragma unroll
-      for (int r=0;r<4;r++)
-        pw[(g*4+r)*40 + t2*16 + l15] = f2bf(sc[nt][r]);
-    }
-    __builtin_amdgcn_wave_barrier();
-    bf16x8 ap = *(const bf16x8*)(pw + l15*40 + g*8);
-    #pragma unroll
-    for (int nd=0;nd<4;nd++){
-      bf16x8 bv = *(const bf16x8*)(vb + (size_t)nd*4096 + kt*32);
-      o[nd] = __builtin_amdgcn_mfma_f32_16x16x32_bf16(ap, bv, o[nd], 0,0,0);
-      if (SPLITV){
-        bf16x8 bl = *(const bf16x8*)(vbl + (size_t)nd*4096 + kt*32);
-        o[nd] = __builtin_amdgcn_mfma_f32_16x16x32_bf16(ap, bl, o[nd], 0,0,0);
-      }
-    }
-  }
-  float inv[4];
-  #pragma unroll
-  for (int r=0;r<4;r++) inv[r] = 1.0f/sum[r];
-  int orow0 = b*nper + q0;
-  #pragma unroll
-  for (int nd=0;nd<4;nd++){
-    #pragma unroll
-    for (int r=0;r<4;r++){
-      float v = o[nd][r]*inv[r];
-      size_t off = (size_t)(orow0 + g*4 + r)*o_rs + h*64 + nd*16 + l15;
-      if (OSPLIT){ unsigned short hh,ll; split2(v,hh,ll); O0[off]=hh; O1[off]=ll; }
-      else O0[off] = f2bf(v);
-    }
-  }
-}
-
-__global__ __launch_bounds__(256) void k_cattn(
-    const float* __restrict__ X, const float* __restrict__ lng, const float* __restrict__ lnb,
-    const unsigned short* __restrict__ WqT, const unsigned short* __restrict__ Kb,
-    const unsigned short* __restrict__ Vt, const unsigned short* __restrict__ WoT,
-    const float* __restrict__ bo, float* __restrict__ C, float scale)
-{
-  __shared__ __align__(16) unsigned short qn[64*40];
-  __shared__ __align__(16) unsigned short qa[4][16*72];
-  int tid = threadIdx.x, lane = tid & 63, w = tid >> 6;
-  int l15 = lane & 15, g = lane >> 4;
-  int r0 = blockIdx.x*64;
-  int bh = r0 >> 14;
-  if (tid < 64){
-    const float* x = X + (size_t)(r0 + tid)*29;
-    float a[29]; float s = 0.f;
-    #pragma unroll
-    for (int k=0;k<29;k++){ a[k]=x[k]; s+=a[k]; }
-    float mean = s*(1.0f/29.0f);
-    float qv = 0.f;
-    #pragma unroll
-    for (int k=0;k<29;k++){ float d=a[k]-mean; qv+=d*d; }
-    float rstd = rsqrtf(qv*(1.0f/29.0f) + 1e-5f);
-    unsigned short yb[32] __attribute__((aligned(16)));
-    #pragma unroll
-    for (int k=0;k<29;k++) yb[k] = f2bf((a[k]-mean)*rstd*lng[k] + lnb[k]);
-    yb[29]=0; yb[30]=0; yb[31]=0;
-    uint4* d4 = (uint4*)(qn + tid*40);
-    const uint4* s4 = (const uint4*)yb;
-    d4[0]=s4[0]; d4[1]=s4[1]; d4[2]=s4[2]; d4[3]=s4[3];
-  }
-  __syncthreads();
-  int rw = w*16;
-  bf16x8 a0 = *(const bf16x8*)(qn + (rw + l15)*40 + g*8);
-  f32x4 qv4[4];
-  #pragma unroll
-  for (int nt=0;nt<4;nt++) qv4[nt] = (f32x4){0.f,0.f,0.f,0.f};
-  #pragma unroll
-  for (int nt=0;nt<4;nt++){
-    bf16x8 bw = *(const bf16x8*)(WqT + (size_t)(nt*16 + l15)*32 + g*8);
-    qv4[nt] = __builtin_amdgcn_mfma_f32_16x16x32_bf16(a0, bw, qv4[nt], 0,0,0);
-  }
-  unsigned short* pa = qa[w];
-  #pragma unroll
-  for (int nt=0;nt<4;nt++)
-    #pragma unroll
-    for (int r=0;r<4;r++)
-      pa[(g*4+r)*72 + nt*16 + l15] = f2bf(qv4[nt][r]);
-  __builtin_amdgcn_wave_barrier();
-  bf16x8 aq[2];
-  aq[0] = *(const bf16x8*)(pa + l15*72 + g*8);
-  aq[1] = *(const bf16x8*)(pa + l15*72 + 32 + g*8);
-  __builtin_amdgcn_wave_barrier();
-  const unsigned short* kbb = Kb + ((size_t)bh*256 + l15)*64 + g*8;
-  f32x4 sc[16];
-  #pragma unroll
-  for (int nt=0;nt<16;nt++) sc[nt] = (f32x4){0.f,0.f,0.f,0.f};
-  #pragma unroll
-  for (int nt=0;nt<16;nt++){
-    bf16x8 b0 = *(const bf16x8*)(kbb + (size_t)nt*1024);
-    bf16x8 b1 = *(const bf16x8*)(kbb + (size_t)nt*1024 + 32);
-    sc[nt] = __builtin_amdgcn_mfma_f32_16x16x32_bf16(aq[0], b0, sc[nt], 0,0,0);
-    sc[nt] = __builtin_amdgcn_mfma_f32_16x16x32_bf16(aq[1], b1, sc[nt], 0,0,0);
-  }
-  float mx[4] = {-1e30f,-1e30f,-1e30f,-1e30f};
-  #pragma unroll
-  for (int nt=0;nt<16;nt++)
-    #pragma unroll
-    for (int r=0;r<4;r++){ float v = sc[nt][r]*scale; sc[nt][r]=v; mx[r]=fmaxf(mx[r],v); }
-  #pragma unroll
-  for (int r=0;r<4;r++){
-    #pragma unroll
-    for (int m=1;m<16;m<<=1) mx[r] = fmaxf(mx[r], __shfl_xor(mx[r], m));
-  }
-  float sum[4] = {0.f,0.f,0.f,0.f};
-  #pragma unroll
-  for (int nt=0;nt<16;nt++)
-    #pragma unroll
-    for (int r=0;r<4;r++){ float e = __expf(sc[nt][r]-mx[r]); sc[nt][r]=e; sum[r]+=e; }
-  #pragma unroll
-  for (int r=0;r<4;r++){
-    #pragma unroll
-    for (int m=1;m<16;m<<=1) sum[r] += __shfl_xor(sum[r], m);
-  }
-  f32x4 o[4];
-  #pragma unroll
-  for (int nd=0;nd<4;nd++) o[nd] = (f32x4){0.f,0.f,0.f,0.f};
-  const unsigned short* vb = Vt + ((size_t)bh*64 + l15)*256 + g*8;
-  #pragma unroll
-  for (int kt=0;kt<8;kt++){
-    __builtin_amdgcn_wave_barrier();
-    #pragma unroll
-    for (int t2=0;t2<2;t2++){
-      int nt = kt*2 + t2;
-      #pragma unroll
-      for (int r=0;r<4;r++)
-        pa[(g*4+r)*40 + t2*16 + l15] = f2bf(sc[nt][r]);
-    }
-    __builtin_amdgcn_wave_barrier();
-    bf16x8 ap = *(const bf16x8*)(pa + l15*40 + g*8);
-    #pragma unroll
-    for (int nd=0;nd<4;nd++){
-      bf16x8 bv = *(const bf16x8*)(vb + (size_t)nd*4096 + kt*32);
-      o[nd] = __builtin_amdgcn_mfma_f32_16x16x32_bf16(ap, bv, o[nd], 0,0,0);
-    }
-  }
-  float inv[4];
-  #pragma unroll
-  for (int r=0;r<4;r++) inv[r] = 1.0f/sum[r];
-  __builtin_amdgcn_wave_barrier();
-  #pragma unroll
-  for (int nd=0;nd<4;nd++)
-    #pragma unroll
-    for (int r=0;r<4;r++)
-      pa[(g*4+r)*72 + nd*16 + l15] = f2bf(o[nd][r]*inv[r]);
-  __builtin_amdgcn_wave_barrier();
-  bf16x8 ao0 = *(const bf16x8*)(pa + l15*72 + g*8);
-  bf16x8 ao1 = *(const bf16x8*)(pa + l15*72 + 32 + g*8);
-  f32x4 c2[2];
-  #pragma unroll
-  for (int nt=0;nt<2;nt++) c2[nt] = (f32x4){0.f,0.f,0.f,0.f};
-  #pragma unroll
-  for (int nt=0;nt<2;nt++){
-    bf16x8 bw0 = *(const bf16x8*)(WoT + (size_t)(nt*16 + l15)*64 + g*8);
-    bf16x8 bw1 = *(const bf16x8*)(WoT + (size_t)(nt*16 + l15)*64 + 32 + g*8);
-    c2[nt] = __builtin_amdgcn_mfma_f32_16x16x32_bf16(ao0, bw0, c2[nt], 0,0,0);
-    c2[nt] = __builtin_amdgcn_mfma_f32_16x16x32_bf16(ao1, bw1, c2[nt], 0,0,0);
-  }
-  #pragma unroll
-  for (int nt=0;nt<2;nt++){
-    int col = nt*16 + l15;
-    if (col < 29){
-      #pragma unroll
-      for (int r=0;r<4;r++){
-        size_t off = (size_t)(r0 + rw + g*4 + r)*29 + col;
-        C[off] += c2[nt][r] + bo[col];
-      }
-    }
-  }
-}
-
-__global__ __launch_bounds__(256) void k_cff(
-    const float* __restrict__ X, const float* __restrict__ lng, const float* __restrict__ lnb,
-    const unsigned short* __restrict__ W1rT, const float* __restrict__ b1r,
-    const unsigned short* __restrict__ W2T, const float* __restrict__ b2,
-    float* __restrict__ C)
-{
-  __shared__ __align__(16) unsigned short sm1[128*40];
-  __shared__ __align__(16) unsigned short gga[4][32*136];
-  int tid = threadIdx.x, lane = tid & 63, w = tid >> 6;
-  int l15 = lane & 15, g = lane >> 4;
-  int row0b = blockIdx.x*128;
-  if (tid < 128){
-    const float* x = X + (size_t)(row0b + tid)*29;
-    float a[29]; float s = 0.f;
-    #pragma unroll
-    for (int k=0;k<29;k++){ a[k]=x[k]; s+=a[k]; }
-    float mean = s*(1.0f/29.0f);
-    float qv = 0.f;
-    #pragma unroll
-    for (int k=0;k<29;k++){ float d=a[k]-mean; qv+=d*d; }
-    float rstd = rsqrtf(qv*(1.0f/29.0f) + 1e-5f);
-    unsigned short yb[32] __attribute__((aligned(16)));
-    #pragma unroll
-    for (int k=0;k<29;k++) yb[k] = f2bf((a[k]-mean)*rstd*lng[k] + lnb[k]);
-    yb[29]=0; yb[30]=0; yb[31]=0;
-    uint4* d4 = (uint4*)(sm1 + tid*40);
-    const uint4* s4 = (const uint4*)yb;
-    d4[0]=s4[0]; d4[1]=s4[1]; d4[2]=s4[2]; d4[3]=s4[3];
-  }
-  __syncthreads();
-  int rw = w*32;
-  bf16x8 a0 = *(const bf16x8*)(sm1 + (rw + l15)*40 + g*8);
-  bf16x8 a1 = *(const bf16x8*)(sm1 + (rw + 16 + l15)*40 + g*8);
-  f32x4 acc[2][16];
-  #pragma unroll
-  for (int mt=0;mt<2;mt++)
-    #pragma unroll
-    for (int nt=0;nt<16;nt++) acc[mt][nt] = (f32x4){0.f,0.f,0.f,0.f};
-  #pragma unroll
-  for (int nt=0;nt<16;nt++){
-    bf16x8 bw = *(const bf16x8*)(W1rT + (size_t)(nt*16 + l15)*32 + g*8);
-    acc[0][nt] = __builtin_amdgcn_mfma_f32_16x16x32_bf16(a0, bw, acc[0][nt], 0,0,0);
-    acc[1][nt] = __builtin_amdgcn_mfma_f32_16x16x32_bf16(a1, bw, acc[1][nt], 0,0,0);
-  }
-  unsigned short* gg = gga[w];
-  #pragma unroll
-  for (int mt=0;mt<2;mt++){
-    #pragma unroll
-    for (int t=0;t<8;t++){
-      float ba = b1r[t*16 + l15];
-      float bg = b1r[128 + t*16 + l15];
-      #pragma unroll
-      for (int r=0;r<4;r++){
-        float av = acc[mt][t][r]   + ba;
-        float gv = acc[mt][t+8][r] + bg;
-        gg[(mt*16 + g*4 + r)*136 + t*16 + l15] = f2bf(av * gelu_exact(gv));
-      }
-    }
-  }
-  __builtin_amdgcn_wave_barrier();
-  f32x4 c2[2][2];
-  #pragma unroll
-  for (int mt=0;mt<2;mt++)
-    #pragma unroll
-    for (int nt=0;nt<2;nt++) c2[mt][nt] = (f32x4){0.f,0.f,0.f,0.f};
-  #pragma unroll
-  for (int kt=0;kt<4;kt++){
-    bf16x8 af0 = *(const bf16x8*)(gg + (size_t)(l15)*136 + kt*32 + g*8);
-    bf16x8 af1 = *(const bf16x8*)(gg + (size_t)(16 + l15)*136 + kt*32 + g*8);
-    #pragma unroll
-    for (int nt=0;nt<2;nt++){
-      bf16x8 bw = *(const bf16x8*)(W2T + (size_t)(nt*16 + l15)*128 + kt*32 + g*8);
-      c2[0][nt] = __builtin_amdgcn_mfma_f32_16x16x32_bf16(af0, bw, c2[0][nt], 0,0,0);
-      c2[1][nt] = __builtin_amdgcn_mfma_f32_16x16x32_bf16(af1, bw, c2[1][nt], 0,0,0);
-    }
-  }
-  #pragma unroll
-  for (int mt=0;mt<2;mt++)
-    #pragma unroll
-    for (int nt=0;nt<2;nt++){
-      int col = nt*16 + l15;
-      if (col < 29){
-        #pragma unroll
-        for (int r=0;r<4;r++){
-          size_t off = (size_t)(row0b + rw + mt*16 + g*4 + r)*29 + col;
-          C[off] += c2[mt][nt][r] + b2[col];
-        }
-      }
-    }
 }
 
 __global__ __launch_bounds__(256) void k_out(const float* __restrict__ data, float* __restrict__ out)
@@ -807,66 +925,64 @@
   float* ws = (float*)d_ws;
   float* data = ws;
   float* lat  = ws + 3801088;
-  unsigned short* latn_hi = (unsigned short*)(ws + 4849664);
-  unsigned short* latn_lo = latn_hi + 1048576;
+  unsigned short* bufA_hi = (unsigned short*)(ws + 4849664);
+  unsigned short* bufA_lo = bufA_hi + 1048576;
   float* I    = ws + 5898240;
+  float* q_l  = I;
+  unsigned short* bufB_hi = (unsigned short*)(I + 1048576);
+  unsigned short* bufB_lo = bufB_hi + 1048576;
+  unsigned short* bufC_hi = (unsigned short*)(I + 2097152);
+  unsigned short* bufC_lo = bufC_hi + 1048576;
+  unsigned short* Kb_l    = (unsigned short*)(I + 3145728);
+  unsigned short* Vthi_l  = Kb_l + 1048576;
+  unsigned short* Vtlo_l  = Vthi_l + 1048576;
+  unsigned short* ao_hi   = (unsigned short*)(I + 4718592);
+  unsigned short* ao_lo   = ao_hi + 1048576;
+  unsigned short* gg_hi   = (unsigned short*)(I + 8388608);
   float* kv_c = ws + 20578304;
   unsigned short* Kb_c = (unsigned short*)(ws + 21626880);
   unsigned short* Vt_c = Kb_c + 131072;
   unsigned short* wsp  = (unsigned short*)(ws + 21757952);
-  float* q_l  = I;
-  unsigned short* Kb_l   = (unsigned short*)(I + 3145728);
-  unsigned short* Vthi_l = Kb_l + 1048576;
-  unsigned short* Vtlo_l = Vthi_l + 1048576;
-  unsigned short* ao_hi  = (unsigned short*)(I + 4718592);
-  unsigned short* ao_lo  = ao_hi + 1048576;
-  unsigned short* gg_hi = (unsigned short*)(I + 8388608);
-  unsigned short* gg_lo = gg_hi + 4194304;
-
-  k_encode<<<64, 256, 0, stream>>>(data);
-  k_l2l   <<<512, 256, 0, stream>>>(x, W_l2l, b_l2l, latents, lat);
-
-  k_split_w<<<dim3(8,8,4),  256,0,stream>>>(la_Wq,  wsp,          512, 512, 1536, 0);
-  k_split_w<<<dim3(8,16,4), 256,0,stream>>>(la_Wkv, wsp,          512,1024, 1536, 512);
-  k_split_w<<<dim3(8,8,4),  256,0,stream>>>(la_Wo,  wsp+1572864,  512, 512,  512, 0);
-  k_split_w<<<dim3(8,64,4), 256,0,stream>>>(lf_W1,  wsp+2097152,  512,4096, 4096, 0);
-  k_split_w<<<dim3(32,8,4), 256,0,stream>>>(lf_W2,  wsp+6291456, 2048, 512,  512, 0);
-  k_split_w<<<dim3(8,2,4),  256,0,stream>>>(ca_Wkv, wsp+8388608,  512, 128,  128, 0);
-  k_prep_t <<<dim3(4,1,4),256,0,stream>>>(ca_Wq, wsp+8519680, 29, 64, 32, 64);
-  k_prep_t <<<dim3(4,1,4),256,0,stream>>>(ca_Wo, wsp+8521728, 64, 29, 64, 32);
-  k_prep_t <<<dim3(8,1,4),256,0,stream>>>(cf_W2, wsp+8523776, 116, 29, 128, 32);
-  k_prep_w1<<<dim3(32,1,4),256,0,stream>>>(cf_W1, cf_b1, wsp+8527872);
-
-  for (int i=0;i<4;i++){
-    unsigned short* wl = wsp + (size_t)i*LSTRIDE;
-    unsigned short* wqkvt= wl;
-    unsigned short* wot  = wl + 1572864;
-    unsigned short* w1t  = wl + 2097152;
-    unsigned short* w2t  = wl + 6291456;
-    unsigned short* cakvt= wl + 8388608;
-    unsigned short* WqT  = wl + 8519680;
-    unsigned short* WoT  = wl + 8521728;
-    unsigned short* W2T  = wl + 8523776;
-    unsigned short* W1rT = wl + 8527872;
-    float* b1r = (float*)(wl + 8536064);
-
-    k_ln512s<<<2048,256,0,stream>>>(lat, la_ln_g+i*512, la_ln_b+i*512, latn_hi, latn_lo);
-    k_mfma_qkv<<<dim3(16,12),256,0,stream>>>(latn_hi, wqkvt, q_l, Kb_l, Vthi_l, Vtlo_l,
-                                             2048, 1536, 512);
-    k_attn_mf<1,1,1><<<256,256,0,stream>>>(q_l, Kb_l, Vthi_l, Vtlo_l, ao_hi, ao_lo,
-                                           512, 512, 8, 256, 0.125f);
-    k_mfma<<<dim3(16,4,2),256,0,stream>>>(ao_hi, wot, la_bo+i*512, lat, 2048, 512, 512, 2, 1);
-    k_ln512s<<<2048,256,0,stream>>>(lat, lf_ln_g+i*512, lf_ln_b+i*512, latn_hi, latn_lo);
-    k_mfma_glu<<<dim3(16,32),256,0,stream>>>(latn_hi, w1t, lf_b1+i*4096, gg_hi, gg_lo);
-    k_mfma<<<dim3(16,4,4),256,0,stream>>>(gg_hi, w2t, lf_b2+i*512, lat, 2048, 512, 2048, 4, 1);
-    k_ln512s<<<2048,256,0,stream>>>(lat, ca_ln_c_g+i*512, ca_ln_c_b+i*512, latn_hi, latn_lo);
-    k_mfma<<<dim3(16,1,4),256,0,stream>>>(latn_hi, cakvt, nullptr, kv_c, 2048, 128, 512, 4, 0);
-    k_kvprep<<<512,256,0,stream>>>(kv_c, 128, 0, 64, 1, 8, Kb_c, Vt_c, nullptr, 4, 262144);
-    k_cattn<<<2048,256,0,stream>>>(data, ca_ln_q_g+i*29, ca_ln_q_b+i*29, WqT,
-                                   Kb_c, Vt_c, WoT, ca_bo+i*29, data, 0.125f);
-    k_cff<<<1024,256,0,stream>>>(data, cf_ln_g+i*29, cf_ln_b+i*29, W1rT, b1r,
-                                 W2T, cf_b2+i*29, data);
-  }
-
-  k_out<<<1536,256,0,stream>>>(data, (float*)d_out);
-}
+
+  k_prep_all<<<4928, 256, 0, stream>>>(x, W_l2l, b_l2l, latents, lat, data,
+      la_Wq, la_Wkv, la_Wo, lf_W1, lf_W2, ca_Wkv, ca_Wq, ca_Wo, cf_W2, cf_W1, cf_b1, wsp);
+  k_ln512w<<<512, 256, 0, stream>>>(lat, la_ln_g, la_ln_b, bufB_hi, bufB_lo);
+
+  for (int i=0;i<5;i++){
+    int li = (i<4)? i : 3;
+    int lx = (i>0)? i-1 : 0;
+    bool L = (i<4), X = (i>0);
+    const unsigned short* wlat = wsp + (size_t)li*LSTRIDE;
+    const unsigned short* wx   = wsp + (size_t)lx*LSTRIDE;
+
+    int nq = L?192:0, nck = X?64:0;
+    k_combo1<<<nq+nck, 256, 0, stream>>>(bufB_hi, wlat, q_l, Kb_l, Vthi_l, Vtlo_l,
+                                         bufA_hi, wx+8388608, kv_c, nq);
+    int na = L?256:0, nkp = X?256:0;
+    k_combo2<<<na+nkp, 256, 0, stream>>>(q_l, Kb_l, Vthi_l, Vtlo_l, ao_hi, ao_lo,
+                                         kv_c, Kb_c, Vt_c, na, nkp);
+    int nwo = L?128:0, nca = X?2048:0;
+    k_combo3<<<nwo+nca, 256, 0, stream>>>(ao_hi, wlat+1572864, la_bo+li*512, lat,
+                                          data, ca_ln_q_g+lx*29, ca_ln_q_b+lx*29,
+                                          wx+8519680, Kb_c, Vt_c, wx+8521728,
+                                          ca_bo+lx*29, nwo);
+    int ncf = X?1024:0, nlf = L?512:0;
+    k_combo4<<<ncf+nlf, 256, 0, stream>>>(data, cf_ln_g+lx*29, cf_ln_b+lx*29,
+                                          wx+8527872, (const float*)(wx+8536064),
+                                          wx+8523776, cf_b2+lx*29,
+                                          lat, lf_ln_g+li*512, lf_ln_b+li*512,
+                                          bufC_hi, bufC_lo, ncf);
+    if (L){
+      k_mfma_glu<<<dim3(16,32), 256, 0, stream>>>(bufC_hi, wlat+2097152, lf_b1+li*4096,
+                                                  gg_hi, gg_hi+4194304);
+      k_mfma<<<dim3(16,4,4), 256, 0, stream>>>(gg_hi, wlat+6291456, lf_b2+li*512, lat,
+                                               2048, 512, 2048, 4, 1);
+      int ln2 = (i<3)? i+1 : 3;
+      k_ln512d<<<512, 256, 0, stream>>>(lat,
+                                        ca_ln_c_g+li*512, ca_ln_c_b+li*512, bufA_hi, bufA_lo,
+                                        la_ln_g+ln2*512, la_ln_b+ln2*512, bufB_hi, bufB_lo);
+    }
+  }
+
+  k_out<<<1536, 256, 0, stream>>>(data, (float*)d_out);
+}
```

Result: faster. 1.552 ms (-16.7%).
